# Kernel tuning notes

Measured on AMD Instinct MI355X. Metric: run time of the kernel, lower is better.

The kernel has to match this reference:

```python
import jax, jax.numpy as jnp
import numpy as np
import math

D_MODEL = 256
D_STATE = 16
DT_RANK = math.ceil(D_MODEL / 16)  # 16
WINDOW = 8
B, S = 2, 1024
LN_EPS = 1e-5


def setup_inputs() -> dict:
    key = jax.random.key(0)
    ks = jax.random.split(key, 24)
    d, n, r = D_MODEL, D_STATE, DT_RANK
    sc = lambda fan_in: 1.0 / math.sqrt(fan_in)
    inp = {
        "x": jax.random.normal(ks[0], (B, S, d), jnp.float32),
        # SelectiveSSM params
        "A_log": jnp.log(jnp.abs(jax.random.normal(ks[1], (d, n))) + 1e-4),
        "W_xproj": jax.random.normal(ks[2], (d, r + n)) * sc(d),
        "W_dt": jax.random.normal(ks[3], (r, d)) * sc(r),
        "b_dt": jnp.zeros((d,)),
        "W_C": jax.random.normal(ks[4], (d, n)) * sc(d),
        # LinearAttentionPathway params
        "Wq": jax.random.normal(ks[5], (d, d)) * sc(d),
        "Wk": jax.random.normal(ks[6], (d, d)) * sc(d),
        "Wv": jax.random.normal(ks[7], (d, d)) * sc(d),
        "Wo": jax.random.normal(ks[8], (d, d)) * sc(d),
        "omega": jax.random.normal(ks[9], (d, d)) * 0.5,  # RFF frequencies (buffer)
        # EntropyGate net: Linear(2d+1 -> d), SiLU, Linear(d -> d), Sigmoid
        "Wg1": jax.random.normal(ks[10], (2 * d + 1, d)) * sc(2 * d + 1),
        "bg1": jnp.zeros((d,)),
        "Wg2": jax.random.normal(ks[11], (d, d)) * sc(d),
        "bg2": jnp.zeros((d,)),
        # LayerNorms
        "ln1_g": jnp.ones((d,)), "ln1_b": jnp.zeros((d,)),
        "ln2_g": jnp.ones((d,)), "ln2_b": jnp.zeros((d,)),
        # FFN (dropout is identity in eval)
        "Wf1": jax.random.normal(ks[12], (d, 4 * d)) * sc(d),
        "bf1": jnp.zeros((4 * d,)),
        "Wf2": jax.random.normal(ks[13], (4 * d, d)) * sc(4 * d),
        "bf2": jnp.zeros((d,)),
    }
    return inp


def _layernorm(x, g, b):
    mu = jnp.mean(x, axis=-1, keepdims=True)
    var = jnp.mean((x - mu) ** 2, axis=-1, keepdims=True)
    return (x - mu) / jnp.sqrt(var + LN_EPS) * g + b


def _ssm(x, A_log, W_xproj, W_dt, b_dt, W_C):
    b, s, d = x.shape
    A = -jnp.exp(A_log)                                   # (d, n)
    xp = x @ W_xproj                                      # (b, s, r+n)
    delta = jax.nn.softplus(xp[..., :DT_RANK] @ W_dt + b_dt)  # (b, s, d)
    Bt = xp[..., DT_RANK:]                                # (b, s, n)
    Ct = x @ W_C                                          # (b, s, n)

    def step(h, ins):
        dlt, B_, C_, x_ = ins                             # (b,d),(b,n),(b,n),(b,d)
        A_bar = jnp.exp(dlt[..., None] * A)               # (b, d, n)
        h = A_bar * h + (dlt * x_)[..., None] * B_[:, None, :]
        y = jnp.einsum('bn,bdn->bd', C_, h)
        return h, y

    xs = (delta.transpose(1, 0, 2), Bt.transpose(1, 0, 2),
          Ct.transpose(1, 0, 2), x.transpose(1, 0, 2))
    h0 = jnp.zeros((b, d, D_STATE), x.dtype)
    _, ys = jax.lax.scan(step, h0, xs)                    # (s, b, d)
    return ys.transpose(1, 0, 2)


def _rff(x, omega):
    proj = x @ omega
    scale = math.sqrt(2.0 / D_MODEL)
    return scale * jnp.concatenate([jnp.cos(proj), jnp.sin(proj)], axis=-1)


def _linear_attn(x, Wq, Wk, Wv, Wo, omega):
    b, s, d = x.shape
    Qp = _rff(x @ Wq, omega)                              # (b, s, 2d)
    Kp = _rff(x @ Wk, omega)                              # (b, s, 2d)
    V = x @ Wv                                            # (b, s, d)
    f = 2 * d

    def step(carry, ins):
        Sm, Z = carry                                     # (b,f,d), (b,f)
        q, k, v = ins
        Sm = Sm + k[..., None] * v[:, None, :]
        Z = Z + k
        num = jnp.einsum('bf,bfd->bd', q, Sm)
        den = jnp.sum(q * Z, axis=-1, keepdims=True)
        return (Sm, Z), num / (den + 1e-6)

    xs = (Qp.transpose(1, 0, 2), Kp.transpose(1, 0, 2), V.transpose(1, 0, 2))
    carry0 = (jnp.zeros((b, f, d), x.dtype), jnp.zeros((b, f), x.dtype))
    _, ys = jax.lax.scan(step, carry0, xs)                # (s, b, d)
    return ys.transpose(1, 0, 2) @ Wo


def _entropy(x):
    # H_t over trailing window of token L2-norms; softmax over window.
    m = jnp.linalg.norm(x, axis=-1)                       # (b, s)
    mp = jnp.pad(m, ((0, 0), (WINDOW - 1, 0)), constant_values=-jnp.inf)
    s = m.shape[1]
    # windows[b, t, w]: norms of positions t-W+1..t (padded with -inf)
    windows = jnp.stack([mp[:, i:i + s] for i in range(WINDOW)], axis=-1)
    p = jax.nn.softmax(windows, axis=-1)                  # -inf pads -> p=0
    H = -jnp.sum(p * (jnp.log(p + 1e-9) / jnp.log(2.0)), axis=-1, keepdims=True)
    return H                                              # (b, s, 1)


def reference(x, A_log, W_xproj, W_dt, b_dt, W_C, Wq, Wk, Wv, Wo, omega,
              Wg1, bg1, Wg2, bg2, ln1_g, ln1_b, ln2_g, ln2_b,
              Wf1, bf1, Wf2, bf2):
    residual = x
    y_ssm = _ssm(x, A_log, W_xproj, W_dt, b_dt, W_C)
    y_attn = _linear_attn(x, Wq, Wk, Wv, Wo, omega)
    H = _entropy(x)
    gate_in = jnp.concatenate([y_ssm, y_attn, H], axis=-1)
    g = jax.nn.sigmoid(jax.nn.silu(gate_in @ Wg1 + bg1) @ Wg2 + bg2)
    y_gated = g * y_ssm + (1.0 - g) * y_attn
    h = _layernorm(residual + y_gated, ln1_g, ln1_b)
    ffn = jax.nn.gelu(h @ Wf1 + bf1, approximate=False) @ Wf2 + bf2
    return _layernorm(h + ffn, ln2_g, ln2_b)
```

## Files before the change

### kernel.cpp

```cpp
#include <hip/hip_runtime.h>
#include <math.h>

typedef unsigned short ushort_t;
typedef unsigned int uint_t;
typedef __attribute__((ext_vector_type(8))) short short8;
typedef __attribute__((ext_vector_type(4))) float f32x4;

#define ACT_NONE     0
#define ACT_SOFTPLUS 1
#define ACT_SILU     2
#define ACT_SIGMOID  3
#define ACT_GELU     4
#define ACT_RFF      5
#define ACT_CAUSAL   6

__device__ __forceinline__ ushort_t f2b(float f) {
    union { float f; uint_t u; } v; v.f = f;
    uint_t u = v.u;
    uint_t r = (u + 0x7FFFu + ((u >> 16) & 1u)) >> 16;
    return (ushort_t)r;
}
__device__ __forceinline__ float b2f(ushort_t h) {
    union { uint_t u; float f; } v; v.u = ((uint_t)h) << 16;
    return v.f;
}
__device__ __forceinline__ void split2(float v, ushort_t& h0, ushort_t& h1) {
    h0 = f2b(v); h1 = f2b(v - b2f(h0));
}
__device__ __forceinline__ void split3(float v, ushort_t& h0, ushort_t& h1, ushort_t& h2) {
    h0 = f2b(v); float r1 = v - b2f(h0);
    h1 = f2b(r1); h2 = f2b(r1 - b2f(h1));
}

__device__ __forceinline__ float fast_erf(float x) {
    float ax = fabsf(x);
    float t = 1.f / (1.f + 0.3275911f * ax);
    float poly = t * (0.254829592f + t * (-0.284496736f + t * (1.421413741f
               + t * (-1.453152027f + t * 1.061405429f))));
    float er = 1.f - poly * __expf(-ax * ax);
    return copysignf(er, x);
}

__device__ __forceinline__ float act_apply(float v, int act) {
    switch (act) {
        case ACT_SOFTPLUS: return v > 0.f ? v + __logf(1.f + __expf(-v)) : __logf(1.f + __expf(v));
        case ACT_SILU:     return v / (1.f + __expf(-v));
        case ACT_SIGMOID:  return 1.f / (1.f + __expf(-v));
        case ACT_GELU:     return 0.5f * v * (1.f + fast_erf(v * 0.7071067811865475f));
        default:           return v;
    }
}

#define LDK2 72
#define TSTRIDE 66

struct GJob {
    const ushort_t *A0, *A1, *A2, *B0, *B1, *B2;
    const float* bias;
    float* outF;
    ushort_t *o0, *o1, *o2, *t0, *t1;
    int lda, ldb, ldo, ldob, colOffB, act, ns, K, N;
    int nx, ny, base, zmod;
    int sAb1, sAb2, sBb1, sBb2, sOb, sObB, sTb;
};

struct SJob {
    const float *x, *delta, *BtCt, *A_log, *hstart;
    float *hend, *Pst;
    ushort_t *giH, *giL;
    int base;
};

template<int NSMAX, int AUXPASS>
__global__ __launch_bounds__(256)
void gemm_multi(GJob J0, GJob J1, GJob J2, GJob J3, GJob J4, SJob S)
{
    __shared__ ushort_t ldsbuf[NSMAX * 2 * 64 * LDK2];
    ushort_t (*sA)[64 * LDK2] = (ushort_t(*)[64 * LDK2])ldsbuf;
    ushort_t (*sB)[64 * LDK2] = (ushort_t(*)[64 * LDK2])(ldsbuf + NSMAX * 64 * LDK2);

    int bid = blockIdx.x;

    if constexpr (AUXPASS != 0) {
        if (bid >= S.base) {
            const int bx2 = bid - S.base;
            const int dblk = bx2 & 15, cc = (bx2 >> 4) & 15, bb2 = bx2 >> 8;
            const int tid2 = threadIdx.x;
            const int nn = tid2 & 15, dl = tid2 >> 4;
            const int dd = dblk * 16 + dl;
            float* sd  = (float*)ldsbuf;
            float* sx2 = sd + 1024;
            float* sB2 = sx2 + 1024;
            float* sC2 = sB2 + 1024;
            #pragma unroll
            for (int it = 0; it < 4; ++it) {
                int i2 = it * 256 + tid2;
                int t2 = i2 >> 4, j2 = i2 & 15;
                long row = (long)bb2 * 1024 + cc * 64 + t2;
                sd[t2 * 16 + j2]  = S.delta[row * 256 + dblk * 16 + j2];
                sx2[t2 * 16 + j2] = S.x[row * 256 + dblk * 16 + j2];
                sB2[t2 * 16 + j2] = S.BtCt[row * 32 + j2];
                if (AUXPASS == 3) sC2[t2 * 16 + j2] = S.BtCt[row * 32 + 16 + j2];
            }
            __syncthreads();
            const float acoef = -__expf(S.A_log[dd * 16 + nn]);
            float h = 0.f, P = 1.f;
            if (AUXPASS == 3) h = S.hstart[((long)(bb2 * 16 + cc) << 12) + dd * 16 + nn];
            for (int t2 = 0; t2 < 64; ++t2) {
                float dlt = sd[t2 * 16 + dl];
                float a2 = __expf(dlt * acoef);
                h = a2 * h + (dlt * sx2[t2 * 16 + dl]) * sB2[t2 * 16 + nn];
                if (AUXPASS == 1) P *= a2;
                if (AUXPASS == 3) {
                    float part = sC2[t2 * 16 + nn] * h;
                    #pragma unroll
                    for (int msk = 8; msk; msk >>= 1) part += __shfl_xor(part, msk, 16);
                    if (nn == 0) {
                        long row = (long)bb2 * 1024 + cc * 64 + t2;
                        ushort_t hh = f2b(part);
                        S.giH[row * 576 + dd] = hh;
                        S.giL[row * 576 + dd] = f2b(part - b2f(hh));
                    }
                }
            }
            if (AUXPASS == 1) {
                long idx = ((long)(bb2 * 16 + cc) << 12) + dd * 16 + nn;
                S.hend[idx] = h;
                S.Pst[idx] = P;
            }
            return;
        }
    }

    GJob J = J0;
    if (J4.nx && bid >= J4.base) J = J4;
    else if (J3.nx && bid >= J3.base) J = J3;
    else if (J2.nx && bid >= J2.base) J = J2;
    else if (J1.nx && bid >= J1.base) J = J1;

    int rel = bid - J.base;
    int perz = J.nx * J.ny;
    int bz = rel / perz; rel -= bz * perz;
    int by = rel / J.nx, bx = rel - by * J.nx;
    int zq = bz / J.zmod, zr = bz - zq * J.zmod;

    const ushort_t* As[3] = {J.A0, J.A1, J.A2};
    const ushort_t* Bs[3] = {J.B0, J.B1, J.B2};
    long offA = (long)zq * J.sAb1 + (long)zr * J.sAb2;
    long offB = (long)zq * J.sBb1 + (long)zr * J.sBb2;
    #pragma unroll
    for (int s = 0; s < NSMAX; ++s) { As[s] += offA; Bs[s] += offB; }
    float* outF = J.outF ? J.outF + (long)bz * J.sOb : nullptr;
    ushort_t* o0 = J.o0 ? J.o0 + (long)bz * J.sObB : nullptr;
    ushort_t* o1 = J.o1 ? J.o1 + (long)bz * J.sObB : nullptr;
    ushort_t* o2 = J.o2 ? J.o2 + (long)bz * J.sObB : nullptr;

    const int m0 = by * 64, n0 = bx * 64;
    const int tid = threadIdx.x, lane = tid & 63, wid = tid >> 6;
    const int wr = (wid >> 1) * 32, wc = (wid & 1) * 32;
    const int lr = lane & 15, lk = (lane >> 4) * 8;
    const int rS = tid >> 3, c8 = (tid & 7) * 8;

    uint4 rA[NSMAX][2], rB[NSMAX][2];

    auto LOAD = [&](int k0) {
        #pragma unroll
        for (int s = 0; s < NSMAX; ++s) if (s < J.ns) {
            #pragma unroll
            for (int p = 0; p < 2; ++p) {
                rA[s][p] = *(const uint4*)(As[s] + (long)(m0 + rS + 32 * p) * J.lda + k0 + c8);
                rB[s][p] = *(const uint4*)(Bs[s] + (long)(n0 + rS + 32 * p) * J.ldb + k0 + c8);
            }
        }
    };
    auto STORE = [&]() {
        #pragma unroll
        for (int s = 0; s < NSMAX; ++s) if (s < J.ns) {
            #pragma unroll
            for (int p = 0; p < 2; ++p) {
                *(uint4*)&sA[s][(rS + 32 * p) * LDK2 + c8] = rA[s][p];
                *(uint4*)&sB[s][(rS + 32 * p) * LDK2 + c8] = rB[s][p];
            }
        }
    };

    f32x4 acc[2][2];
    #pragma unroll
    for (int i = 0; i < 2; ++i)
        #pragma unroll
        for (int j = 0; j < 2; ++j)
            acc[i][j] = (f32x4){0.f, 0.f, 0.f, 0.f};

    const int niter = J.K >> 6;
    LOAD(0);
    for (int it = 0; it < niter; ++it) {
        if (it) __syncthreads();
        STORE();
        __syncthreads();
        if (it + 1 < niter) LOAD((it + 1) << 6);
        #pragma unroll
        for (int ks = 0; ks < 2; ++ks) {
            short8 af[NSMAX][2], bg[NSMAX][2];
            #pragma unroll
            for (int s = 0; s < NSMAX; ++s) if (s < J.ns) {
                af[s][0] = *(const short8*)&sA[s][(wr + lr) * LDK2 + ks * 32 + lk];
                af[s][1] = *(const short8*)&sA[s][(wr + 16 + lr) * LDK2 + ks * 32 + lk];
                bg[s][0] = *(const short8*)&sB[s][(wc + lr) * LDK2 + ks * 32 + lk];
                bg[s][1] = *(const short8*)&sB[s][(wc + 16 + lr) * LDK2 + ks * 32 + lk];
            }
            #pragma unroll
            for (int i = 0; i < 2; ++i) {
                #pragma unroll
                for (int j = 0; j < 2; ++j) {
                    acc[i][j] = __builtin_amdgcn_mfma_f32_16x16x32_bf16(af[0][i], bg[0][j], acc[i][j], 0, 0, 0);
                    if constexpr (NSMAX >= 2) if (J.ns >= 2) {
                        acc[i][j] = __builtin_amdgcn_mfma_f32_16x16x32_bf16(af[0][i], bg[1][j], acc[i][j], 0, 0, 0);
                        acc[i][j] = __builtin_amdgcn_mfma_f32_16x16x32_bf16(af[1][i], bg[0][j], acc[i][j], 0, 0, 0);
                    }
                    if constexpr (NSMAX >= 3) if (J.ns >= 3) {
                        acc[i][j] = __builtin_amdgcn_mfma_f32_16x16x32_bf16(af[0][i], bg[2][j], acc[i][j], 0, 0, 0);
                        acc[i][j] = __builtin_amdgcn_mfma_f32_16x16x32_bf16(af[1][i], bg[1][j], acc[i][j], 0, 0, 0);
                        acc[i][j] = __builtin_amdgcn_mfma_f32_16x16x32_bf16(af[2][i], bg[0][j], acc[i][j], 0, 0, 0);
                    }
                }
            }
        }
    }

    ushort_t* sAf = &sA[0][0];
    ushort_t* sBf = &sB[0][0];
    const bool hasT = (J.t0 != nullptr);
    if (hasT) __syncthreads();

    #pragma unroll
    for (int i = 0; i < 2; ++i) {
        #pragma unroll
        for (int j = 0; j < 2; ++j) {
            #pragma unroll
            for (int rr = 0; rr < 4; ++rr) {
                int rl2 = wr + i * 16 + (lane >> 4) * 4 + rr;
                int cl2 = wc + j * 16 + lr;
                int row = m0 + rl2;
                int col = n0 + cl2;
                if (col >= J.N) continue;
                float v = acc[i][j][rr];
                if (J.bias) v += J.bias[col];
                if (J.act == ACT_RFF) {
                    const float sc = 0.08838834764831845f;
                    float sv_, cv_;
                    __sincosf(v, &sv_, &cv_);
                    float cv = sc * cv_, sv = sc * sv_;
                    ushort_t ch = f2b(cv), sh = f2b(sv);
                    ushort_t cL = f2b(cv - b2f(ch)), sL = f2b(sv - b2f(sh));
                    long oc = (long)row * J.ldob + col, os = oc + J.N;
                    o0[oc] = ch; o0[os] = sh;
                    o1[oc] = cL; o1[os] = sL;
                    if (hasT) {
                        sAf[cl2 * TSTRIDE + rl2] = ch;
                        sAf[4224 + cl2 * TSTRIDE + rl2] = cL;
                        sBf[cl2 * TSTRIDE + rl2] = sh;
                        sBf[4224 + cl2 * TSTRIDE + rl2] = sL;
                    }
                    continue;
                }
                if (J.act == ACT_CAUSAL) { if (col > row) v = 0.f; }
                else v = act_apply(v, J.act);
                if (outF) outF[(long)row * J.ldo + col] = v;
                if (o0) {
                    long o = (long)row * J.ldob + J.colOffB + col;
                    ushort_t h0 = f2b(v); o0[o] = h0;
                    if (o1) {
                        float r1 = v - b2f(h0);
                        ushort_t h1 = f2b(r1); o1[o] = h1;
                        if (o2) o2[o] = f2b(r1 - b2f(h1));
                    }
                }
                if (hasT) {
                    ushort_t h0 = f2b(v);
                    sAf[cl2 * TSTRIDE + rl2] = h0;
                    sAf[4224 + cl2 * TSTRIDE + rl2] = f2b(v - b2f(h0));
                }
            }
        }
    }

    if (hasT) {
        __syncthreads();
        int bb = m0 >> 10, tl0 = m0 & 1023;
        int cl = tid >> 2, seg = tid & 3;
        int ngroups = (J.act == ACT_RFF) ? 2 : 1;
        for (int g = 0; g < ngroups; ++g) {
            const ushort_t* th = (g ? sBf : sAf) + cl * TSTRIDE + seg * 16;
            const ushort_t* tl = th + 4224;
            long gcol = (long)(n0 + cl) + (long)g * J.N;
            long addr = (long)bb * J.sTb + gcol * 1024 + tl0 + seg * 16;
            uint_t wh[8], wl[8];
            #pragma unroll
            for (int k2 = 0; k2 < 8; ++k2) {
                wh[k2] = (uint_t)th[2 * k2] | ((uint_t)th[2 * k2 + 1] << 16);
                wl[k2] = (uint_t)tl[2 * k2] | ((uint_t)tl[2 * k2 + 1] << 16);
            }
            *(uint4*)(J.t0 + addr)     = *(uint4*)&wh[0];
            *(uint4*)(J.t0 + addr + 8) = *(uint4*)&wh[4];
            *(uint4*)(J.t1 + addr)     = *(uint4*)&wl[0];
            *(uint4*)(J.t1 + addr + 8) = *(uint4*)&wl[4];
        }
    }
}

#define CONV_BLKS 6400
__global__ __launch_bounds__(256)
void convert_kernel(const float* __restrict__ x, const float* __restrict__ Wxp,
                    const float* __restrict__ Wdt, const float* __restrict__ Wc,
                    const float* __restrict__ Wq, const float* __restrict__ Wk,
                    const float* __restrict__ Wv, const float* __restrict__ Wo,
                    const float* __restrict__ omega, const float* __restrict__ Wg1,
                    const float* __restrict__ Wg2, const float* __restrict__ Wf1,
                    const float* __restrict__ Wf2,
                    ushort_t* x0, ushort_t* x1, ushort_t* x2,
                    ushort_t* omT0, ushort_t* omT1, ushort_t* omT2,
                    ushort_t* Wq0, ushort_t* Wq1, ushort_t* Wq2,
                    ushort_t* Wk0, ushort_t* Wk1, ushort_t* Wk2,
                    ushort_t* WvT0, ushort_t* WvT1, ushort_t* WoT0, ushort_t* WoT1,
                    ushort_t* Wg1T0, ushort_t* Wg1T1, ushort_t* Wg2T0, ushort_t* Wg2T1,
                    ushort_t* Wf1T, ushort_t* Wf2T,
                    ushort_t* WdtT0, ushort_t* WdtT1, ushort_t* WxpP0, ushort_t* WxpP1,
                    ushort_t* WbcT0, ushort_t* WbcT1, float* mbuf)
{
    if (blockIdx.x >= CONV_BLKS) {
        int w = threadIdx.x >> 6, lane = threadIdx.x & 63;
        int token = (blockIdx.x - CONV_BLKS) * 4 + w;
        const float4 v = ((const float4*)(x + (long)token * 256))[lane];
        float s = v.x * v.x + v.y * v.y + v.z * v.z + v.w * v.w;
        #pragma unroll
        for (int msk = 32; msk; msk >>= 1) s += __shfl_xor(s, msk, 64);
        if (lane == 0) mbuf[token] = sqrtf(s);
        return;
    }
    int i = blockIdx.x * 256 + threadIdx.x;
    if (i < 524288) { split3(x[i], x0[i], x1[i], x2[i]); return; }
    i -= 524288;
    if (i < 65536) { int r = i >> 8, c = i & 255; split3(omega[c * 256 + r], omT0[i], omT1[i], omT2[i]); return; }
    i -= 65536;
    if (i < 65536) { split3(Wq[i], Wq0[i], Wq1[i], Wq2[i]); return; }
    i -= 65536;
    if (i < 65536) { split3(Wk[i], Wk0[i], Wk1[i], Wk2[i]); return; }
    i -= 65536;
    if (i < 65536) { int r = i >> 8, c = i & 255; split2(Wv[c * 256 + r], WvT0[i], WvT1[i]); return; }
    i -= 65536;
    if (i < 65536) { int r = i >> 8, c = i & 255; split2(Wo[c * 256 + r], WoT0[i], WoT1[i]); return; }
    i -= 65536;
    if (i < 147456) { int r = i / 576, c = i - r * 576;
                      float v = (c < 513) ? Wg1[c * 256 + r] : 0.f;
                      split2(v, Wg1T0[i], Wg1T1[i]); return; }
    i -= 147456;
    if (i < 65536) { int r = i >> 8, c = i & 255; split2(Wg2[c * 256 + r], Wg2T0[i], Wg2T1[i]); return; }
    i -= 65536;
    if (i < 262144) { int r = i >> 8, c = i & 255; Wf1T[i] = f2b(Wf1[c * 1024 + r]); return; }
    i -= 262144;
    if (i < 262144) { int r = i >> 10, c = i & 1023; Wf2T[i] = f2b(Wf2[c * 256 + r]); return; }
    i -= 262144;
    if (i < 16384) { int m = i >> 6, k = i & 63;
                     float v = (k < 16) ? Wdt[k * 256 + m] : 0.f;
                     split2(v, WdtT0[i], WdtT1[i]); return; }
    i -= 16384;
    if (i < 16384) { int n = i >> 6, k = i & 63;
                     float v = (k < 16) ? Wxp[n * 32 + k] : 0.f;
                     split2(v, WxpP0[i], WxpP1[i]); return; }
    i -= 16384;
    if (i < 16384) { int r = i >> 8, c = i & 255;
                     float v = (r < 16) ? Wxp[c * 32 + 16 + r] : ((r < 32) ? Wc[c * 16 + (r - 16)] : 0.f);
                     split2(v, WbcT0[i], WbcT1[i]); return; }
}

__global__ void scan_mix(const float* __restrict__ hend, const float* __restrict__ Pst,
                         float* __restrict__ hstart,
                         const ushort_t* __restrict__ Kh, const ushort_t* __restrict__ Kl,
                         float* __restrict__ dzc,
                         const float* __restrict__ dST,
                         ushort_t* __restrict__ STh, ushort_t* __restrict__ STl)
{
    int gb = blockIdx.x;
    if (gb < 32) {
        int tid = gb * 256 + threadIdx.x;
        int b = tid >> 12;
        int dn = tid & 4095;
        float hs = 0.f;
        for (int c = 0; c < 16; ++c) {
            long idx = ((long)(b * 16 + c) << 12) + dn;
            hstart[idx] = hs;
            hs = Pst[idx] * hs + hend[idx];
        }
    } else if (gb < 64) {
        int idx = (gb - 32) * 256 + threadIdx.x;
        int bc = idx >> 9, f = idx & 511;
        float s = 0.f;
        for (int t = 0; t < 128; ++t) {
            long i = ((long)bc * 128 + t) * 512 + f;
            s += b2f(Kh[i]) + b2f(Kl[i]);
        }
        dzc[(long)bc * 512 + f] = s;
    } else {
        int t = (gb - 64) * 256 + threadIdx.x;
        int b = t >> 17;
        int df = t & 131071;
        float acc = 0.f;
        for (int c = 0; c < 8; ++c) {
            long idx = (long)(b * 8 + c) * 131072 + df;
            float v = dST[idx];
            ushort_t h = f2b(acc);
            STh[idx] = h;
            STl[idx] = f2b(acc - b2f(h));
            acc += v;
        }
    }
}

__global__ void attn_finish(const float* __restrict__ scores,
                            const ushort_t* __restrict__ Qh, const ushort_t* __restrict__ Ql,
                            const float* __restrict__ dzc,
                            const float* __restrict__ numA, const float* __restrict__ numB,
                            const float* __restrict__ mbuf,
                            ushort_t* __restrict__ yh, ushort_t* __restrict__ yl,
                            ushort_t* __restrict__ giH, ushort_t* __restrict__ giL)
{
    int token = blockIdx.x;
    int b = token >> 10, tloc = token & 1023;
    int c = tloc >> 7, tin = tloc & 127;
    int bc = b * 8 + c;
    int lane = threadIdx.x;
    const float* srow = scores + ((long)bc * 128 + tin) * 128;
    float s = srow[lane] + srow[lane + 64];
    const ushort_t* qh = Qh + (long)token * 512;
    const ushort_t* ql = Ql + (long)token * 512;
    float q[8];
    #pragma unroll
    for (int j = 0; j < 8; ++j) {
        int f = lane + 64 * j;
        q[j] = b2f(qh[f]) + b2f(ql[f]);
    }
    for (int c2 = 0; c2 < c; ++c2) {
        const float* z = dzc + (long)(b * 8 + c2) * 512;
        #pragma unroll
        for (int j = 0; j < 8; ++j) s += q[j] * z[lane + 64 * j];
    }
    #pragma unroll
    for (int m = 32; m; m >>= 1) s += __shfl_xor(s, m, 64);
    float inv = 1.f / (s + 1e-6f);
    const float* na = numA + (long)token * 256;
    const float* nb = numB + (long)token * 256;
    #pragma unroll
    for (int j = 0; j < 4; ++j) {
        int idx = lane + 64 * j;
        float v = (na[idx] + nb[idx]) * inv;
        ushort_t h = f2b(v);
        yh[(long)token * 256 + idx] = h;
        yl[(long)token * 256 + idx] = f2b(v - b2f(h));
    }
    if (lane == 0) {
        float w[8];
        #pragma unroll
        for (int i = 0; i < 8; ++i) {
            int idx = tloc - 7 + i;
            w[i] = (idx >= 0) ? mbuf[b * 1024 + idx] : -1e30f;
        }
        float mx = w[0];
        #pragma unroll
        for (int i = 1; i < 8; ++i) mx = fmaxf(mx, w[i]);
        float e[8], sum = 0.f;
        #pragma unroll
        for (int i = 0; i < 8; ++i) { e[i] = __expf(w[i] - mx); sum += e[i]; }
        float invs = 1.f / sum, Hv = 0.f;
        #pragma unroll
        for (int i = 0; i < 8; ++i) {
            float p = e[i] * invs;
            Hv -= p * __logf(p + 1e-9f);
        }
        float H = Hv * 1.4426950408889634f;
        ushort_t hh = f2b(H);
        giH[(long)token * 576 + 512] = hh;
        giL[(long)token * 576 + 512] = f2b(H - b2f(hh));
    }
    if (lane < 63) {
        giH[(long)token * 576 + 513 + lane] = 0;
        giL[(long)token * 576 + 513 + lane] = 0;
    }
}

__global__ __launch_bounds__(256)
void ln1_kernel(const float* __restrict__ x, const float* __restrict__ g,
                const ushort_t* __restrict__ giH, const ushort_t* __restrict__ giL,
                const float* __restrict__ gamma, const float* __restrict__ beta,
                float* __restrict__ outF, ushort_t* __restrict__ outB)
{
    __shared__ float red[8];
    long t = blockIdx.x;
    int i = threadIdx.x;
    long idx = t * 256 + i;
    float yssm  = b2f(giH[t * 576 + i])       + b2f(giL[t * 576 + i]);
    float yattn = b2f(giH[t * 576 + 256 + i]) + b2f(giL[t * 576 + 256 + i]);
    float gv = g[idx];
    float v = x[idx] + gv * yssm + (1.f - gv) * yattn;
    float s = v;
    #pragma unroll
    for (int m = 32; m; m >>= 1) s += __shfl_xor(s, m, 64);
    if ((i & 63) == 0) red[i >> 6] = s;
    __syncthreads();
    float mu = (red[0] + red[1] + red[2] + red[3]) * (1.f / 256.f);
    float dv = v - mu;
    float s2 = dv * dv;
    #pragma unroll
    for (int m = 32; m; m >>= 1) s2 += __shfl_xor(s2, m, 64);
    if ((i & 63) == 0) red[4 + (i >> 6)] = s2;
    __syncthreads();
    float var = (red[4] + red[5] + red[6] + red[7]) * (1.f / 256.f);
    float o = dv * rsqrtf(var + 1e-5f) * gamma[i] + beta[i];
    outF[idx] = o;
    outB[idx] = f2b(o);
}

__global__ __launch_bounds__(256)
void ln2_kernel(const float* __restrict__ h, const float* __restrict__ f2,
                const float* __restrict__ gamma, const float* __restrict__ beta,
                float* __restrict__ out)
{
    __shared__ float red[8];
    long t = blockIdx.x;
    int i = threadIdx.x;
    long idx = t * 256 + i;
    float v = h[idx] + f2[idx];
    float s = v;
    #pragma unroll
    for (int m = 32; m; m >>= 1) s += __shfl_xor(s, m, 64);
    if ((i & 63) == 0) red[i >> 6] = s;
    __syncthreads();
    float mu = (red[0] + red[1] + red[2] + red[3]) * (1.f / 256.f);
    float dv = v - mu;
    float s2 = dv * dv;
    #pragma unroll
    for (int m = 32; m; m >>= 1) s2 += __shfl_xor(s2, m, 64);
    if ((i & 63) == 0) red[4 + (i >> 6)] = s2;
    __syncthreads();
    float var = (red[4] + red[5] + red[6] + red[7]) * (1.f / 256.f);
    out[idx] = dv * rsqrtf(var + 1e-5f) * gamma[i] + beta[i];
}


extern "C" void kernel_launch(void* const* d_in, const int* in_sizes, int n_in,
                              void* d_out, int out_size, void* d_ws, size_t ws_size,
                              hipStream_t stream)
{
    const float* x       = (const float*)d_in[0];
    const float* A_log   = (const float*)d_in[1];
    const float* W_xproj = (const float*)d_in[2];
    const float* W_dt    = (const float*)d_in[3];
    const float* b_dt    = (const float*)d_in[4];
    const float* W_C     = (const float*)d_in[5];
    const float* Wq      = (const float*)d_in[6];
    const float* Wk      = (const float*)d_in[7];
    const float* Wv      = (const float*)d_in[8];
    const float* Wo      = (const float*)d_in[9];
    const float* omega   = (const float*)d_in[10];
    const float* Wg1     = (const float*)d_in[11];
    const float* bg1     = (const float*)d_in[12];
    const float* Wg2     = (const float*)d_in[13];
    const float* bg2     = (const float*)d_in[14];
    const float* ln1_g   = (const float*)d_in[15];
    const float* ln1_b   = (const float*)d_in[16];
    const float* ln2_g   = (const float*)d_in[17];
    const float* ln2_b   = (const float*)d_in[18];
    const float* Wf1     = (const float*)d_in[19];
    const float* bf1     = (const float*)d_in[20];
    const float* Wf2     = (const float*)d_in[21];
    const float* bf2     = (const float*)d_in[22];

    char* B = (char*)d_ws;
    float* out = (float*)d_out;
    if (ws_size < (size_t)42778624) return;

    ushort_t* x0      = (ushort_t*)(B + 0);
    ushort_t* x1      = (ushort_t*)(B + 1048576);
    ushort_t* x2      = (ushort_t*)(B + 2097152);
    ushort_t* Qp_hi   = (ushort_t*)(B + 3145728);
    ushort_t* Qp_lo   = (ushort_t*)(B + 5242880);
    ushort_t* Kp_hi   = (ushort_t*)(B + 7340032);
    ushort_t* Kp_lo   = (ushort_t*)(B + 9437184);
    ushort_t* KpT_hi  = (ushort_t*)(B + 11534336);
    ushort_t* KpT_lo  = (ushort_t*)(B + 13631488);
    ushort_t* VT_hi   = (ushort_t*)(B + 15728640);
    ushort_t* VT_lo   = (ushort_t*)(B + 16777216);
    float*    dST_f   = (float*)(B + 17825792);
    float*    delta_f = (float*)(B + 26214400);
    float*    BtCt_f  = (float*)(B + 28311552);
    ushort_t* Wg1T0   = (ushort_t*)(B + 28573696);
    ushort_t* Wg1T1   = (ushort_t*)(B + 28868608);
    ushort_t* Wf1T    = (ushort_t*)(B + 29163520);
    ushort_t* Wf2T    = (ushort_t*)(B + 29687808);
    ushort_t* WxdT0   = (ushort_t*)(B + 30212096);
    ushort_t* WxdT1   = (ushort_t*)(B + 30343168);
    ushort_t* WvT0    = (ushort_t*)(B + 30474240);
    ushort_t* WvT1    = (ushort_t*)(B + 30605312);
    ushort_t* WoT0    = (ushort_t*)(B + 30736384);
    ushort_t* WoT1    = (ushort_t*)(B + 30867456);
    ushort_t* Wg2T0   = (ushort_t*)(B + 30998528);
    ushort_t* Wg2T1   = (ushort_t*)(B + 31129600);
    ushort_t* WdtT0   = (ushort_t*)(B + 31260672);
    ushort_t* WdtT1   = (ushort_t*)(B + 31293440);
    ushort_t* WxpP0   = (ushort_t*)(B + 31326208);
    ushort_t* WxpP1   = (ushort_t*)(B + 31358976);
    ushort_t* WbcT0   = (ushort_t*)(B + 31391744);
    ushort_t* WbcT1   = (ushort_t*)(B + 31424512);
    float*    mbuf    = (float*)(B + 31457280);
    float*    dzc     = (float*)(B + 31465472);
    ushort_t* gatein_hi = (ushort_t*)(B + 31498240);
    ushort_t* gatein_lo = (ushort_t*)(B + 33857536);
    ushort_t* ST_lo   = (ushort_t*)(B + 36216832);
    float*    scores_f  = (float*)(B + 40411136);
    ushort_t* scores_hi = (ushort_t*)(B + 41459712);
    ushort_t* scores_lo = (ushort_t*)(B + 41984000);
    ushort_t* omT0  = (ushort_t*)(B + 17825792);
    ushort_t* omT1  = (ushort_t*)(B + 17956864);
    ushort_t* omT2  = (ushort_t*)(B + 18087936);
    ushort_t* Wq0   = (ushort_t*)(B + 18219008);
    ushort_t* Wq1   = (ushort_t*)(B + 18350080);
    ushort_t* Wq2   = (ushort_t*)(B + 18481152);
    ushort_t* Wk0   = (ushort_t*)(B + 18612224);
    ushort_t* Wk1   = (ushort_t*)(B + 18743296);
    ushort_t* Wk2   = (ushort_t*)(B + 18874368);
    ushort_t* WqoT0 = (ushort_t*)(B + 19005440);
    ushort_t* WqoT1 = (ushort_t*)(B + 19136512);
    ushort_t* WqoT2 = (ushort_t*)(B + 19267584);
    ushort_t* WkoT0 = (ushort_t*)(B + 19398656);
    ushort_t* WkoT1 = (ushort_t*)(B + 19529728);
    ushort_t* WkoT2 = (ushort_t*)(B + 19660800);
    ushort_t* ST_hi = (ushort_t*)(B + 11534336);
    float*    hend   = (float*)(B + 0);
    float*    Pst    = (float*)(B + 524288);
    float*    hstart = (float*)(B + 1048576);
    float*    numA_f = (float*)(B + 17825792);
    float*    numB_f = (float*)(B + 19922944);
    ushort_t* g1_hi  = (ushort_t*)(B + 22020096);
    ushort_t* g1_lo  = (ushort_t*)(B + 23068672);
    float*    gbuf_f = (float*)(B + 24117248);
    ushort_t* ypre_hi = (ushort_t*)(B + 7340032);
    ushort_t* ypre_lo = (ushort_t*)(B + 8388608);
    float*    hbuf_f  = (float*)(B + 11534336);
    ushort_t* hbuf_b  = (ushort_t*)(B + 13631488);
    ushort_t* ffn1_b  = (ushort_t*)(B + 3145728);
    float*    ffn2_f  = (float*)(B + 15728640);

    dim3 T256(256);
    GJob jz{};
    SJob sz{};

    convert_kernel<<<dim3(CONV_BLKS + 512), T256, 0, stream>>>(x, W_xproj, W_dt, W_C,
        Wq, Wk, Wv, Wo, omega, Wg1, Wg2, Wf1, Wf2,
        x0, x1, x2, omT0, omT1, omT2, Wq0, Wq1, Wq2, Wk0, Wk1, Wk2,
        WvT0, WvT1, WoT0, WoT1, Wg1T0, Wg1T1, Wg2T0, Wg2T1, Wf1T, Wf2T,
        WdtT0, WdtT1, WxpP0, WxpP1, WbcT0, WbcT1, mbuf);

    {
        GJob a{}; a.A0=omT0; a.A1=omT1; a.A2=omT2; a.B0=Wq0; a.B1=Wq1; a.B2=Wq2;
        a.o0=WqoT0; a.o1=WqoT1; a.o2=WqoT2; a.lda=256; a.ldb=256; a.ldob=256;
        a.act=ACT_NONE; a.ns=3; a.K=256; a.N=256; a.nx=4; a.ny=4; a.base=0; a.zmod=1;
        GJob b = a; b.B0=Wk0; b.B1=Wk1; b.B2=Wk2; b.o0=WkoT0; b.o1=WkoT1; b.o2=WkoT2; b.base=16;
        GJob c{}; c.A0=WdtT0; c.A1=WdtT1; c.B0=WxpP0; c.B1=WxpP1;
        c.o0=WxdT0; c.o1=WxdT1; c.lda=64; c.ldb=64; c.ldob=256;
        c.act=ACT_NONE; c.ns=2; c.K=64; c.N=256; c.nx=4; c.ny=4; c.base=32; c.zmod=1;
        gemm_multi<3,0><<<dim3(48), T256, 0, stream>>>(a, b, c, jz, jz, sz);
    }
    {
        GJob v{}; v.A0=x0; v.A1=x1; v.B0=WvT0; v.B1=WvT1;
        v.t0=VT_hi; v.t1=VT_lo; v.sTb=262144;
        v.lda=256; v.ldb=256; v.act=ACT_NONE; v.ns=2; v.K=256; v.N=256;
        v.nx=4; v.ny=32; v.base=0; v.zmod=1;
        GJob q{}; q.A0=x0; q.A1=x1; q.A2=x2; q.B0=WqoT0; q.B1=WqoT1; q.B2=WqoT2;
        q.o0=Qp_hi; q.o1=Qp_lo; q.lda=256; q.ldb=256; q.ldob=512;
        q.act=ACT_RFF; q.ns=3; q.K=256; q.N=256; q.nx=4; q.ny=32; q.base=128; q.zmod=1;
        GJob k = q; k.B0=WkoT0; k.B1=WkoT1; k.B2=WkoT2; k.o0=Kp_hi; k.o1=Kp_lo;
        k.t0=KpT_hi; k.t1=KpT_lo; k.sTb=524288; k.base=256;
        GJob bc{}; bc.A0=x0; bc.A1=x1; bc.B0=WbcT0; bc.B1=WbcT1;
        bc.outF=BtCt_f; bc.lda=256; bc.ldb=256; bc.ldo=32;
        bc.act=ACT_NONE; bc.ns=2; bc.K=256; bc.N=32; bc.nx=1; bc.ny=32; bc.base=384; bc.zmod=1;
        GJob dl{}; dl.A0=x0; dl.A1=x1; dl.B0=WxdT0; dl.B1=WxdT1; dl.bias=b_dt;
        dl.outF=delta_f; dl.lda=256; dl.ldb=256; dl.ldo=256;
        dl.act=ACT_SOFTPLUS; dl.ns=2; dl.K=256; dl.N=256; dl.nx=4; dl.ny=32; dl.base=416; dl.zmod=1;
        gemm_multi<3,0><<<dim3(544), T256, 0, stream>>>(v, q, k, bc, dl, sz);
    }
    {
        GJob d{}; d.A0=VT_hi; d.A1=VT_lo; d.B0=KpT_hi; d.B1=KpT_lo;
        d.outF=dST_f; d.lda=1024; d.ldb=1024; d.ldo=512;
        d.act=ACT_NONE; d.ns=2; d.K=128; d.N=512; d.nx=8; d.ny=4; d.base=0; d.zmod=8;
        d.sAb1=262144; d.sAb2=128; d.sBb1=524288; d.sBb2=128; d.sOb=131072;
        GJob s{}; s.A0=Qp_hi; s.A1=Qp_lo; s.B0=Kp_hi; s.B1=Kp_lo;
        s.outF=scores_f; s.o0=scores_hi; s.o1=scores_lo;
        s.lda=512; s.ldb=512; s.ldo=128; s.ldob=128;
        s.act=ACT_CAUSAL; s.ns=2; s.K=512; s.N=128; s.nx=2; s.ny=2; s.base=512; s.zmod=1;
        s.sAb1=65536; s.sBb1=65536; s.sOb=16384; s.sObB=16384;
        SJob s1{}; s1.x=x; s1.delta=delta_f; s1.BtCt=BtCt_f; s1.A_log=A_log;
        s1.hend=hend; s1.Pst=Pst; s1.base=576;
        gemm_multi<2,1><<<dim3(1088), T256, 0, stream>>>(d, s, jz, jz, jz, s1);
    }
    scan_mix<<<dim3(1088), T256, 0, stream>>>(hend, Pst, hstart, Kp_hi, Kp_lo, dzc,
                                              dST_f, ST_hi, ST_lo);
    {
        GJob a{}; a.A0=scores_hi; a.A1=scores_lo; a.B0=VT_hi; a.B1=VT_lo;
        a.outF=numA_f; a.lda=128; a.ldb=1024; a.ldo=256;
        a.act=ACT_NONE; a.ns=2; a.K=128; a.N=256; a.nx=4; a.ny=2; a.base=0; a.zmod=8;
        a.sAb1=131072; a.sAb2=16384; a.sBb1=262144; a.sBb2=128; a.sOb=32768;
        GJob b{}; b.A0=Qp_hi; b.A1=Qp_lo; b.B0=ST_hi; b.B1=ST_lo;
        b.outF=numB_f; b.lda=512; b.ldb=512; b.ldo=256;
        b.act=ACT_NONE; b.ns=2; b.K=512; b.N=256; b.nx=4; b.ny=2; b.base=128; b.zmod=1;
        b.sAb1=65536; b.sBb1=131072; b.sOb=32768;
        SJob s3{}; s3.x=x; s3.delta=delta_f; s3.BtCt=BtCt_f; s3.A_log=A_log;
        s3.hstart=hstart; s3.giH=gatein_hi; s3.giL=gatein_lo; s3.base=256;
        gemm_multi<2,3><<<dim3(768), T256, 0, stream>>>(a, b, jz, jz, jz, s3);
    }
    attn_finish<<<dim3(2048), dim3(64), 0, stream>>>(scores_f, Qp_hi, Qp_lo, dzc,
        numA_f, numB_f, mbuf, ypre_hi, ypre_lo, gatein_hi, gatein_lo);
    {
        GJob w{}; w.A0=ypre_hi; w.A1=ypre_lo; w.B0=WoT0; w.B1=WoT1;
        w.o0=gatein_hi; w.o1=gatein_lo; w.colOffB=256;
        w.lda=256; w.ldb=256; w.ldob=576;
        w.act=ACT_NONE; w.ns=2; w.K=256; w.N=256; w.nx=4; w.ny=32; w.base=0; w.zmod=1;
        gemm_multi<2,0><<<dim3(128), T256, 0, stream>>>(w, jz, jz, jz, jz, sz);
    }
    {
        GJob g{}; g.A0=gatein_hi; g.A1=gatein_lo; g.B0=Wg1T0; g.B1=Wg1T1; g.bias=bg1;
        g.o0=g1_hi; g.o1=g1_lo; g.lda=576; g.ldb=576; g.ldob=256;
        g.act=ACT_SILU; g.ns=2; g.K=576; g.N=256; g.nx=4; g.ny=32; g.base=0; g.zmod=1;
        gemm_multi<2,0><<<dim3(128), T256, 0, stream>>>(g, jz, jz, jz, jz, sz);
    }
    {
        GJob g{}; g.A0=g1_hi; g.A1=g1_lo; g.B0=Wg2T0; g.B1=Wg2T1; g.bias=bg2;
        g.outF=gbuf_f; g.lda=256; g.ldb=256; g.ldo=256;
        g.act=ACT_SIGMOID; g.ns=2; g.K=256; g.N=256; g.nx=4; g.ny=32; g.base=0; g.zmod=1;
        gemm_multi<2,0><<<dim3(128), T256, 0, stream>>>(g, jz, jz, jz, jz, sz);
    }
    ln1_kernel<<<dim3(2048), T256, 0, stream>>>(x, gbuf_f, gatein_hi, gatein_lo, ln1_g, ln1_b, hbuf_f, hbuf_b);
    {
        GJob f{}; f.A0=hbuf_b; f.B0=Wf1T; f.bias=bf1;
        f.o0=ffn1_b; f.lda=256; f.ldb=256; f.ldob=1024;
        f.act=ACT_GELU; f.ns=1; f.K=256; f.N=1024; f.nx=16; f.ny=32; f.base=0; f.zmod=1;
        gemm_multi<1,0><<<dim3(512), T256, 0, stream>>>(f, jz, jz, jz, jz, sz);
    }
    {
        GJob f{}; f.A0=ffn1_b; f.B0=Wf2T; f.bias=bf2;
        f.outF=ffn2_f; f.lda=1024; f.ldb=1024; f.ldo=256;
        f.act=ACT_NONE; f.ns=1; f.K=1024; f.N=256; f.nx=4; f.ny=32; f.base=0; f.zmod=1;
        gemm_multi<1,0><<<dim3(128), T256, 0, stream>>>(f, jz, jz, jz, jz, sz);
    }
    ln2_kernel<<<dim3(2048), T256, 0, stream>>>(hbuf_f, ffn2_f, ln2_g, ln2_b, out);
}
```

Before: 311.8 us.

## Fuse all stages into one cooperative persistent kernel with grid syncs

Replaces the chain of separate kernel launches (convert, multi-GEMMs, scans, attention finish, gate GEMMs, layernorms, FFN) with a single cooperative persistent kernel. Blocks loop over virtual block IDs in each stage, and stages are separated by grid.sync(). This targets launch overhead and inter-kernel gaps across roughly a dozen dependent launches. In exchange it limits the grid to 256 or 512 resident blocks, which may reduce parallelism for stages that had many more blocks. Each grid-wide barrier also has its own cost.

```diff
diff --git a/kernel.cpp b/kernel.cpp
--- a/kernel.cpp
+++ b/kernel.cpp
@@ -1,5 +1,8 @@
 #include <hip/hip_runtime.h>
+#include <hip/hip_cooperative_groups.h>
 #include <math.h>
+
+namespace cg = cooperative_groups;
 
 typedef unsigned short ushort_t;
 typedef unsigned int uint_t;
@@ -64,79 +67,14 @@
     int sAb1, sAb2, sBb1, sBb2, sOb, sObB, sTb;
 };
 
-struct SJob {
-    const float *x, *delta, *BtCt, *A_log, *hstart;
-    float *hend, *Pst;
-    ushort_t *giH, *giL;
-    int base;
-};
-
-template<int NSMAX, int AUXPASS>
-__global__ __launch_bounds__(256)
-void gemm_multi(GJob J0, GJob J1, GJob J2, GJob J3, GJob J4, SJob S)
+template<int NSMAX>
+__device__ __noinline__ void gemm_body(int bid, const GJob* js, int nj, ushort_t* ldsbuf)
 {
-    __shared__ ushort_t ldsbuf[NSMAX * 2 * 64 * LDK2];
     ushort_t (*sA)[64 * LDK2] = (ushort_t(*)[64 * LDK2])ldsbuf;
     ushort_t (*sB)[64 * LDK2] = (ushort_t(*)[64 * LDK2])(ldsbuf + NSMAX * 64 * LDK2);
 
-    int bid = blockIdx.x;
-
-    if constexpr (AUXPASS != 0) {
-        if (bid >= S.base) {
-            const int bx2 = bid - S.base;
-            const int dblk = bx2 & 15, cc = (bx2 >> 4) & 15, bb2 = bx2 >> 8;
-            const int tid2 = threadIdx.x;
-            const int nn = tid2 & 15, dl = tid2 >> 4;
-            const int dd = dblk * 16 + dl;
-            float* sd  = (float*)ldsbuf;
-            float* sx2 = sd + 1024;
-            float* sB2 = sx2 + 1024;
-            float* sC2 = sB2 + 1024;
-            #pragma unroll
-            for (int it = 0; it < 4; ++it) {
-                int i2 = it * 256 + tid2;
-                int t2 = i2 >> 4, j2 = i2 & 15;
-                long row = (long)bb2 * 1024 + cc * 64 + t2;
-                sd[t2 * 16 + j2]  = S.delta[row * 256 + dblk * 16 + j2];
-                sx2[t2 * 16 + j2] = S.x[row * 256 + dblk * 16 + j2];
-                sB2[t2 * 16 + j2] = S.BtCt[row * 32 + j2];
-                if (AUXPASS == 3) sC2[t2 * 16 + j2] = S.BtCt[row * 32 + 16 + j2];
-            }
-            __syncthreads();
-            const float acoef = -__expf(S.A_log[dd * 16 + nn]);
-            float h = 0.f, P = 1.f;
-            if (AUXPASS == 3) h = S.hstart[((long)(bb2 * 16 + cc) << 12) + dd * 16 + nn];
-            for (int t2 = 0; t2 < 64; ++t2) {
-                float dlt = sd[t2 * 16 + dl];
-                float a2 = __expf(dlt * acoef);
-                h = a2 * h + (dlt * sx2[t2 * 16 + dl]) * sB2[t2 * 16 + nn];
-                if (AUXPASS == 1) P *= a2;
-                if (AUXPASS == 3) {
-                    float part = sC2[t2 * 16 + nn] * h;
-                    #pragma unroll
-                    for (int msk = 8; msk; msk >>= 1) part += __shfl_xor(part, msk, 16);
-                    if (nn == 0) {
-                        long row = (long)bb2 * 1024 + cc * 64 + t2;
-                        ushort_t hh = f2b(part);
-                        S.giH[row * 576 + dd] = hh;
-                        S.giL[row * 576 + dd] = f2b(part - b2f(hh));
-                    }
-                }
-            }
-            if (AUXPASS == 1) {
-                long idx = ((long)(bb2 * 16 + cc) << 12) + dd * 16 + nn;
-                S.hend[idx] = h;
-                S.Pst[idx] = P;
-            }
-            return;
-        }
-    }
-
-    GJob J = J0;
-    if (J4.nx && bid >= J4.base) J = J4;
-    else if (J3.nx && bid >= J3.base) J = J3;
-    else if (J2.nx && bid >= J2.base) J = J2;
-    else if (J1.nx && bid >= J1.base) J = J1;
+    GJob J = js[0];
+    for (int j = nj - 1; j > 0; --j) if (bid >= js[j].base) { J = js[j]; break; }
 
     int rel = bid - J.base;
     int perz = J.nx * J.ny;
@@ -306,358 +244,165 @@
             *(uint4*)(J.t1 + addr + 8) = *(uint4*)&wl[4];
         }
     }
-}
-
-#define CONV_BLKS 6400
-__global__ __launch_bounds__(256)
-void convert_kernel(const float* __restrict__ x, const float* __restrict__ Wxp,
-                    const float* __restrict__ Wdt, const float* __restrict__ Wc,
-                    const float* __restrict__ Wq, const float* __restrict__ Wk,
-                    const float* __restrict__ Wv, const float* __restrict__ Wo,
-                    const float* __restrict__ omega, const float* __restrict__ Wg1,
-                    const float* __restrict__ Wg2, const float* __restrict__ Wf1,
-                    const float* __restrict__ Wf2,
-                    ushort_t* x0, ushort_t* x1, ushort_t* x2,
-                    ushort_t* omT0, ushort_t* omT1, ushort_t* omT2,
-                    ushort_t* Wq0, ushort_t* Wq1, ushort_t* Wq2,
-                    ushort_t* Wk0, ushort_t* Wk1, ushort_t* Wk2,
-                    ushort_t* WvT0, ushort_t* WvT1, ushort_t* WoT0, ushort_t* WoT1,
-                    ushort_t* Wg1T0, ushort_t* Wg1T1, ushort_t* Wg2T0, ushort_t* Wg2T1,
-                    ushort_t* Wf1T, ushort_t* Wf2T,
-                    ushort_t* WdtT0, ushort_t* WdtT1, ushort_t* WxpP0, ushort_t* WxpP1,
-                    ushort_t* WbcT0, ushort_t* WbcT1, float* mbuf)
+    __syncthreads();
+}
+
+template<int PASS>
+__device__ __noinline__ void ssm_body(int bx2, const float* x, const float* delta,
+                                      const float* BtCt, const float* A_log,
+                                      float* hend, float* Pst, const float* hstart,
+                                      ushort_t* giH, ushort_t* giL, ushort_t* ldsbuf)
 {
-    if (blockIdx.x >= CONV_BLKS) {
-        int w = threadIdx.x >> 6, lane = threadIdx.x & 63;
-        int token = (blockIdx.x - CONV_BLKS) * 4 + w;
-        const float4 v = ((const float4*)(x + (long)token * 256))[lane];
-        float s = v.x * v.x + v.y * v.y + v.z * v.z + v.w * v.w;
-        #pragma unroll
-        for (int msk = 32; msk; msk >>= 1) s += __shfl_xor(s, msk, 64);
-        if (lane == 0) mbuf[token] = sqrtf(s);
-        return;
-    }
-    int i = blockIdx.x * 256 + threadIdx.x;
-    if (i < 524288) { split3(x[i], x0[i], x1[i], x2[i]); return; }
-    i -= 524288;
-    if (i < 65536) { int r = i >> 8, c = i & 255; split3(omega[c * 256 + r], omT0[i], omT1[i], omT2[i]); return; }
-    i -= 65536;
-    if (i < 65536) { split3(Wq[i], Wq0[i], Wq1[i], Wq2[i]); return; }
-    i -= 65536;
-    if (i < 65536) { split3(Wk[i], Wk0[i], Wk1[i], Wk2[i]); return; }
-    i -= 65536;
-    if (i < 65536) { int r = i >> 8, c = i & 255; split2(Wv[c * 256 + r], WvT0[i], WvT1[i]); return; }
-    i -= 65536;
-    if (i < 65536) { int r = i >> 8, c = i & 255; split2(Wo[c * 256 + r], WoT0[i], WoT1[i]); return; }
-    i -= 65536;
-    if (i < 147456) { int r = i / 576, c = i - r * 576;
-                      float v = (c < 513) ? Wg1[c * 256 + r] : 0.f;
-                      split2(v, Wg1T0[i], Wg1T1[i]); return; }
-    i -= 147456;
-    if (i < 65536) { int r = i >> 8, c = i & 255; split2(Wg2[c * 256 + r], Wg2T0[i], Wg2T1[i]); return; }
-    i -= 65536;
-    if (i < 262144) { int r = i >> 8, c = i & 255; Wf1T[i] = f2b(Wf1[c * 1024 + r]); return; }
-    i -= 262144;
-    if (i < 262144) { int r = i >> 10, c = i & 1023; Wf2T[i] = f2b(Wf2[c * 256 + r]); return; }
-    i -= 262144;
-    if (i < 16384) { int m = i >> 6, k = i & 63;
-                     float v = (k < 16) ? Wdt[k * 256 + m] : 0.f;
-                     split2(v, WdtT0[i], WdtT1[i]); return; }
-    i -= 16384;
-    if (i < 16384) { int n = i >> 6, k = i & 63;
-                     float v = (k < 16) ? Wxp[n * 32 + k] : 0.f;
-                     split2(v, WxpP0[i], WxpP1[i]); return; }
-    i -= 16384;
-    if (i < 16384) { int r = i >> 8, c = i & 255;
-                     float v = (r < 16) ? Wxp[c * 32 + 16 + r] : ((r < 32) ? Wc[c * 16 + (r - 16)] : 0.f);
-                     split2(v, WbcT0[i], WbcT1[i]); return; }
-}
-
-__global__ void scan_mix(const float* __restrict__ hend, const float* __restrict__ Pst,
-                         float* __restrict__ hstart,
-                         const ushort_t* __restrict__ Kh, const ushort_t* __restrict__ Kl,
-                         float* __restrict__ dzc,
-                         const float* __restrict__ dST,
-                         ushort_t* __restrict__ STh, ushort_t* __restrict__ STl)
+    const int dblk = bx2 & 15, cc = (bx2 >> 4) & 15, bb2 = bx2 >> 8;
+    const int tid2 = threadIdx.x;
+    const int nn = tid2 & 15, dl = tid2 >> 4;
+    const int dd = dblk * 16 + dl;
+    float* sd  = (float*)ldsbuf;
+    float* sx2 = sd + 1024;
+    float* sB2 = sx2 + 1024;
+    float* sC2 = sB2 + 1024;
+    #pragma unroll
+    for (int it = 0; it < 4; ++it) {
+        int i2 = it * 256 + tid2;
+        int t2 = i2 >> 4, j2 = i2 & 15;
+        long row = (long)bb2 * 1024 + cc * 64 + t2;
+        sd[t2 * 16 + j2]  = delta[row * 256 + dblk * 16 + j2];
+        sx2[t2 * 16 + j2] = x[row * 256 + dblk * 16 + j2];
+        sB2[t2 * 16 + j2] = BtCt[row * 32 + j2];
+        if (PASS == 3) sC2[t2 * 16 + j2] = BtCt[row * 32 + 16 + j2];
+    }
+    __syncthreads();
+    const float acoef = -__expf(A_log[dd * 16 + nn]);
+    float h = 0.f, P = 1.f;
+    if (PASS == 3) h = hstart[((long)(bb2 * 16 + cc) << 12) + dd * 16 + nn];
+    for (int t2 = 0; t2 < 64; ++t2) {
+        float dlt = sd[t2 * 16 + dl];
+        float a2 = __expf(dlt * acoef);
+        h = a2 * h + (dlt * sx2[t2 * 16 + dl]) * sB2[t2 * 16 + nn];
+        if (PASS == 1) P *= a2;
+        if (PASS == 3) {
+            float part = sC2[t2 * 16 + nn] * h;
+            #pragma unroll
+            for (int msk = 8; msk; msk >>= 1) part += __shfl_xor(part, msk, 16);
+            if (nn == 0) {
+                long row = (long)bb2 * 1024 + cc * 64 + t2;
+                ushort_t hh = f2b(part);
+                giH[row * 576 + dd] = hh;
+                giL[row * 576 + dd] = f2b(part - b2f(hh));
+            }
+        }
+    }
+    if (PASS == 1) {
+        long idx = ((long)(bb2 * 16 + cc) << 12) + dd * 16 + nn;
+        hend[idx] = h;
+        Pst[idx] = P;
+    }
+    __syncthreads();
+}
+
+struct MegaArgs {
+    const float *x, *A_log, *Wxp, *Wdt, *b_dt, *Wc, *Wq, *Wk, *Wv, *Wo, *omega,
+                *Wg1, *bg1, *Wg2, *bg2, *ln1g, *ln1b, *ln2g, *ln2b,
+                *Wf1, *bf1, *Wf2, *bf2;
+    char* B;
+    float* out;
+};
+
+#define PUS(off) ((ushort_t*)(A.B + (off)))
+#define PF(off)  ((float*)(A.B + (off)))
+
+__global__ void __launch_bounds__(256)
+mega(MegaArgs A)
 {
-    int gb = blockIdx.x;
-    if (gb < 32) {
-        int tid = gb * 256 + threadIdx.x;
-        int b = tid >> 12;
-        int dn = tid & 4095;
-        float hs = 0.f;
-        for (int c = 0; c < 16; ++c) {
-            long idx = ((long)(b * 16 + c) << 12) + dn;
-            hstart[idx] = hs;
-            hs = Pst[idx] * hs + hend[idx];
-        }
-    } else if (gb < 64) {
-        int idx = (gb - 32) * 256 + threadIdx.x;
-        int bc = idx >> 9, f = idx & 511;
-        float s = 0.f;
-        for (int t = 0; t < 128; ++t) {
-            long i = ((long)bc * 128 + t) * 512 + f;
-            s += b2f(Kh[i]) + b2f(Kl[i]);
-        }
-        dzc[(long)bc * 512 + f] = s;
-    } else {
-        int t = (gb - 64) * 256 + threadIdx.x;
-        int b = t >> 17;
-        int df = t & 131071;
-        float acc = 0.f;
-        for (int c = 0; c < 8; ++c) {
-            long idx = (long)(b * 8 + c) * 131072 + df;
-            float v = dST[idx];
-            ushort_t h = f2b(acc);
-            STh[idx] = h;
-            STl[idx] = f2b(acc - b2f(h));
-            acc += v;
-        }
-    }
-}
-
-__global__ void attn_finish(const float* __restrict__ scores,
-                            const ushort_t* __restrict__ Qh, const ushort_t* __restrict__ Ql,
-                            const float* __restrict__ dzc,
-                            const float* __restrict__ numA, const float* __restrict__ numB,
-                            const float* __restrict__ mbuf,
-                            ushort_t* __restrict__ yh, ushort_t* __restrict__ yl,
-                            ushort_t* __restrict__ giH, ushort_t* __restrict__ giL)
-{
-    int token = blockIdx.x;
-    int b = token >> 10, tloc = token & 1023;
-    int c = tloc >> 7, tin = tloc & 127;
-    int bc = b * 8 + c;
-    int lane = threadIdx.x;
-    const float* srow = scores + ((long)bc * 128 + tin) * 128;
-    float s = srow[lane] + srow[lane + 64];
-    const ushort_t* qh = Qh + (long)token * 512;
-    const ushort_t* ql = Ql + (long)token * 512;
-    float q[8];
-    #pragma unroll
-    for (int j = 0; j < 8; ++j) {
-        int f = lane + 64 * j;
-        q[j] = b2f(qh[f]) + b2f(ql[f]);
-    }
-    for (int c2 = 0; c2 < c; ++c2) {
-        const float* z = dzc + (long)(b * 8 + c2) * 512;
-        #pragma unroll
-        for (int j = 0; j < 8; ++j) s += q[j] * z[lane + 64 * j];
-    }
-    #pragma unroll
-    for (int m = 32; m; m >>= 1) s += __shfl_xor(s, m, 64);
-    float inv = 1.f / (s + 1e-6f);
-    const float* na = numA + (long)token * 256;
-    const float* nb = numB + (long)token * 256;
-    #pragma unroll
-    for (int j = 0; j < 4; ++j) {
-        int idx = lane + 64 * j;
-        float v = (na[idx] + nb[idx]) * inv;
-        ushort_t h = f2b(v);
-        yh[(long)token * 256 + idx] = h;
-        yl[(long)token * 256 + idx] = f2b(v - b2f(h));
-    }
-    if (lane == 0) {
-        float w[8];
-        #pragma unroll
-        for (int i = 0; i < 8; ++i) {
-            int idx = tloc - 7 + i;
-            w[i] = (idx >= 0) ? mbuf[b * 1024 + idx] : -1e30f;
-        }
-        float mx = w[0];
-        #pragma unroll
-        for (int i = 1; i < 8; ++i) mx = fmaxf(mx, w[i]);
-        float e[8], sum = 0.f;
-        #pragma unroll
-        for (int i = 0; i < 8; ++i) { e[i] = __expf(w[i] - mx); sum += e[i]; }
-        float invs = 1.f / sum, Hv = 0.f;
-        #pragma unroll
-        for (int i = 0; i < 8; ++i) {
-            float p = e[i] * invs;
-            Hv -= p * __logf(p + 1e-9f);
-        }
-        float H = Hv * 1.4426950408889634f;
-        ushort_t hh = f2b(H);
-        giH[(long)token * 576 + 512] = hh;
-        giL[(long)token * 576 + 512] = f2b(H - b2f(hh));
-    }
-    if (lane < 63) {
-        giH[(long)token * 576 + 513 + lane] = 0;
-        giL[(long)token * 576 + 513 + lane] = 0;
-    }
-}
-
-__global__ __launch_bounds__(256)
-void ln1_kernel(const float* __restrict__ x, const float* __restrict__ g,
-                const ushort_t* __restrict__ giH, const ushort_t* __restrict__ giL,
-                const float* __restrict__ gamma, const float* __restrict__ beta,
-                float* __restrict__ outF, ushort_t* __restrict__ outB)
-{
-    __shared__ float red[8];
-    long t = blockIdx.x;
-    int i = threadIdx.x;
-    long idx = t * 256 + i;
-    float yssm  = b2f(giH[t * 576 + i])       + b2f(giL[t * 576 + i]);
-    float yattn = b2f(giH[t * 576 + 256 + i]) + b2f(giL[t * 576 + 256 + i]);
-    float gv = g[idx];
-    float v = x[idx] + gv * yssm + (1.f - gv) * yattn;
-    float s = v;
-    #pragma unroll
-    for (int m = 32; m; m >>= 1) s += __shfl_xor(s, m, 64);
-    if ((i & 63) == 0) red[i >> 6] = s;
-    __syncthreads();
-    float mu = (red[0] + red[1] + red[2] + red[3]) * (1.f / 256.f);
-    float dv = v - mu;
-    float s2 = dv * dv;
-    #pragma unroll
-    for (int m = 32; m; m >>= 1) s2 += __shfl_xor(s2, m, 64);
-    if ((i & 63) == 0) red[4 + (i >> 6)] = s2;
-    __syncthreads();
-    float var = (red[4] + red[5] + red[6] + red[7]) * (1.f / 256.f);
-    float o = dv * rsqrtf(var + 1e-5f) * gamma[i] + beta[i];
-    outF[idx] = o;
-    outB[idx] = f2b(o);
-}
-
-__global__ __launch_bounds__(256)
-void ln2_kernel(const float* __restrict__ h, const float* __restrict__ f2,
-                const float* __restrict__ gamma, const float* __restrict__ beta,
-                float* __restrict__ out)
-{
-    __shared__ float red[8];
-    long t = blockIdx.x;
-    int i = threadIdx.x;
-    long idx = t * 256 + i;
-    float v = h[idx] + f2[idx];
-    float s = v;
-    #pragma unroll
-    for (int m = 32; m; m >>= 1) s += __shfl_xor(s, m, 64);
-    if ((i & 63) == 0) red[i >> 6] = s;
-    __syncthreads();
-    float mu = (red[0] + red[1] + red[2] + red[3]) * (1.f / 256.f);
-    float dv = v - mu;
-    float s2 = dv * dv;
-    #pragma unroll
-    for (int m = 32; m; m >>= 1) s2 += __shfl_xor(s2, m, 64);
-    if ((i & 63) == 0) red[4 + (i >> 6)] = s2;
-    __syncthreads();
-    float var = (red[4] + red[5] + red[6] + red[7]) * (1.f / 256.f);
-    out[idx] = dv * rsqrtf(var + 1e-5f) * gamma[i] + beta[i];
-}
-
-
-extern "C" void kernel_launch(void* const* d_in, const int* in_sizes, int n_in,
-                              void* d_out, int out_size, void* d_ws, size_t ws_size,
-                              hipStream_t stream)
-{
-    const float* x       = (const float*)d_in[0];
-    const float* A_log   = (const float*)d_in[1];
-    const float* W_xproj = (const float*)d_in[2];
-    const float* W_dt    = (const float*)d_in[3];
-    const float* b_dt    = (const float*)d_in[4];
-    const float* W_C     = (const float*)d_in[5];
-    const float* Wq      = (const float*)d_in[6];
-    const float* Wk      = (const float*)d_in[7];
-    const float* Wv      = (const float*)d_in[8];
-    const float* Wo      = (const float*)d_in[9];
-    const float* omega   = (const float*)d_in[10];
-    const float* Wg1     = (const float*)d_in[11];
-    const float* bg1     = (const float*)d_in[12];
-    const float* Wg2     = (const float*)d_in[13];
-    const float* bg2     = (const float*)d_in[14];
-    const float* ln1_g   = (const float*)d_in[15];
-    const float* ln1_b   = (const float*)d_in[16];
-    const float* ln2_g   = (const float*)d_in[17];
-    const float* ln2_b   = (const float*)d_in[18];
-    const float* Wf1     = (const float*)d_in[19];
-    const float* bf1     = (const float*)d_in[20];
-    const float* Wf2     = (const float*)d_in[21];
-    const float* bf2     = (const float*)d_in[22];
-
-    char* B = (char*)d_ws;
-    float* out = (float*)d_out;
-    if (ws_size < (size_t)42778624) return;
-
-    ushort_t* x0      = (ushort_t*)(B + 0);
-    ushort_t* x1      = (ushort_t*)(B + 1048576);
-    ushort_t* x2      = (ushort_t*)(B + 2097152);
-    ushort_t* Qp_hi   = (ushort_t*)(B + 3145728);
-    ushort_t* Qp_lo   = (ushort_t*)(B + 5242880);
-    ushort_t* Kp_hi   = (ushort_t*)(B + 7340032);
-    ushort_t* Kp_lo   = (ushort_t*)(B + 9437184);
-    ushort_t* KpT_hi  = (ushort_t*)(B + 11534336);
-    ushort_t* KpT_lo  = (ushort_t*)(B + 13631488);
-    ushort_t* VT_hi   = (ushort_t*)(B + 15728640);
-    ushort_t* VT_lo   = (ushort_t*)(B + 16777216);
-    float*    dST_f   = (float*)(B + 17825792);
-    float*    delta_f = (float*)(B + 26214400);
-    float*    BtCt_f  = (float*)(B + 28311552);
-    ushort_t* Wg1T0   = (ushort_t*)(B + 28573696);
-    ushort_t* Wg1T1   = (ushort_t*)(B + 28868608);
-    ushort_t* Wf1T    = (ushort_t*)(B + 29163520);
-    ushort_t* Wf2T    = (ushort_t*)(B + 29687808);
-    ushort_t* WxdT0   = (ushort_t*)(B + 30212096);
-    ushort_t* WxdT1   = (ushort_t*)(B + 30343168);
-    ushort_t* WvT0    = (ushort_t*)(B + 30474240);
-    ushort_t* WvT1    = (ushort_t*)(B + 30605312);
-    ushort_t* WoT0    = (ushort_t*)(B + 30736384);
-    ushort_t* WoT1    = (ushort_t*)(B + 30867456);
-    ushort_t* Wg2T0   = (ushort_t*)(B + 30998528);
-    ushort_t* Wg2T1   = (ushort_t*)(B + 31129600);
-    ushort_t* WdtT0   = (ushort_t*)(B + 31260672);
-    ushort_t* WdtT1   = (ushort_t*)(B + 31293440);
-    ushort_t* WxpP0   = (ushort_t*)(B + 31326208);
-    ushort_t* WxpP1   = (ushort_t*)(B + 31358976);
-    ushort_t* WbcT0   = (ushort_t*)(B + 31391744);
-    ushort_t* WbcT1   = (ushort_t*)(B + 31424512);
-    float*    mbuf    = (float*)(B + 31457280);
-    float*    dzc     = (float*)(B + 31465472);
-    ushort_t* gatein_hi = (ushort_t*)(B + 31498240);
-    ushort_t* gatein_lo = (ushort_t*)(B + 33857536);
-    ushort_t* ST_lo   = (ushort_t*)(B + 36216832);
-    float*    scores_f  = (float*)(B + 40411136);
-    ushort_t* scores_hi = (ushort_t*)(B + 41459712);
-    ushort_t* scores_lo = (ushort_t*)(B + 41984000);
-    ushort_t* omT0  = (ushort_t*)(B + 17825792);
-    ushort_t* omT1  = (ushort_t*)(B + 17956864);
-    ushort_t* omT2  = (ushort_t*)(B + 18087936);
-    ushort_t* Wq0   = (ushort_t*)(B + 18219008);
-    ushort_t* Wq1   = (ushort_t*)(B + 18350080);
-    ushort_t* Wq2   = (ushort_t*)(B + 18481152);
-    ushort_t* Wk0   = (ushort_t*)(B + 18612224);
-    ushort_t* Wk1   = (ushort_t*)(B + 18743296);
-    ushort_t* Wk2   = (ushort_t*)(B + 18874368);
-    ushort_t* WqoT0 = (ushort_t*)(B + 19005440);
-    ushort_t* WqoT1 = (ushort_t*)(B + 19136512);
-    ushort_t* WqoT2 = (ushort_t*)(B + 19267584);
-    ushort_t* WkoT0 = (ushort_t*)(B + 19398656);
-    ushort_t* WkoT1 = (ushort_t*)(B + 19529728);
-    ushort_t* WkoT2 = (ushort_t*)(B + 19660800);
-    ushort_t* ST_hi = (ushort_t*)(B + 11534336);
-    float*    hend   = (float*)(B + 0);
-    float*    Pst    = (float*)(B + 524288);
-    float*    hstart = (float*)(B + 1048576);
-    float*    numA_f = (float*)(B + 17825792);
-    float*    numB_f = (float*)(B + 19922944);
-    ushort_t* g1_hi  = (ushort_t*)(B + 22020096);
-    ushort_t* g1_lo  = (ushort_t*)(B + 23068672);
-    float*    gbuf_f = (float*)(B + 24117248);
-    ushort_t* ypre_hi = (ushort_t*)(B + 7340032);
-    ushort_t* ypre_lo = (ushort_t*)(B + 8388608);
-    float*    hbuf_f  = (float*)(B + 11534336);
-    ushort_t* hbuf_b  = (ushort_t*)(B + 13631488);
-    ushort_t* ffn1_b  = (ushort_t*)(B + 3145728);
-    float*    ffn2_f  = (float*)(B + 15728640);
-
-    dim3 T256(256);
-    GJob jz{};
-    SJob sz{};
-
-    convert_kernel<<<dim3(CONV_BLKS + 512), T256, 0, stream>>>(x, W_xproj, W_dt, W_C,
-        Wq, Wk, Wv, Wo, omega, Wg1, Wg2, Wf1, Wf2,
-        x0, x1, x2, omT0, omT1, omT2, Wq0, Wq1, Wq2, Wk0, Wk1, Wk2,
-        WvT0, WvT1, WoT0, WoT1, Wg1T0, Wg1T1, Wg2T0, Wg2T1, Wf1T, Wf2T,
-        WdtT0, WdtT1, WxpP0, WxpP1, WbcT0, WbcT1, mbuf);
+    cg::grid_group grid = cg::this_grid();
+    __shared__ ushort_t ldsbuf[3 * 2 * 64 * LDK2];
+    const int NB = gridDim.x;
+    const int bid = blockIdx.x;
+    const int tid = threadIdx.x;
+
+    ushort_t *x0 = PUS(0), *x1 = PUS(1048576), *x2 = PUS(2097152);
+    ushort_t *Qp_hi = PUS(3145728), *Qp_lo = PUS(5242880);
+    ushort_t *Kp_hi = PUS(7340032), *Kp_lo = PUS(9437184);
+    ushort_t *KpT_hi = PUS(11534336), *KpT_lo = PUS(13631488);
+    ushort_t *VT_hi = PUS(15728640), *VT_lo = PUS(16777216);
+    float *dST_f = PF(17825792), *delta_f = PF(26214400), *BtCt_f = PF(28311552);
+    ushort_t *Wg1T0 = PUS(28573696), *Wg1T1 = PUS(28868608);
+    ushort_t *Wf1T = PUS(29163520), *Wf2T = PUS(29687808);
+    ushort_t *WxdT0 = PUS(30212096), *WxdT1 = PUS(30343168);
+    ushort_t *WvT0 = PUS(30474240), *WvT1 = PUS(30605312);
+    ushort_t *WoT0 = PUS(30736384), *WoT1 = PUS(30867456);
+    ushort_t *Wg2T0 = PUS(30998528), *Wg2T1 = PUS(31129600);
+    ushort_t *WdtT0 = PUS(31260672), *WdtT1 = PUS(31293440);
+    ushort_t *WxpP0 = PUS(31326208), *WxpP1 = PUS(31358976);
+    ushort_t *WbcT0 = PUS(31391744), *WbcT1 = PUS(31424512);
+    float *mbuf = PF(31457280), *dzc = PF(31465472);
+    ushort_t *gatein_hi = PUS(31498240), *gatein_lo = PUS(33857536);
+    ushort_t *ST_lo = PUS(36216832);
+    float *scores_f = PF(40411136);
+    ushort_t *scores_hi = PUS(41459712), *scores_lo = PUS(41984000);
+    ushort_t *omT0 = PUS(17825792), *omT1 = PUS(17956864), *omT2 = PUS(18087936);
+    ushort_t *Wq0 = PUS(18219008), *Wq1 = PUS(18350080), *Wq2 = PUS(18481152);
+    ushort_t *Wk0 = PUS(18612224), *Wk1 = PUS(18743296), *Wk2 = PUS(18874368);
+    ushort_t *WqoT0 = PUS(19005440), *WqoT1 = PUS(19136512), *WqoT2 = PUS(19267584);
+    ushort_t *WkoT0 = PUS(19398656), *WkoT1 = PUS(19529728), *WkoT2 = PUS(19660800);
+    ushort_t *ST_hi = PUS(11534336);
+    float *hend = PF(0), *Pst = PF(524288), *hstart = PF(1048576);
+    float *numA_f = PF(17825792), *numB_f = PF(19922944);
+    ushort_t *g1_hi = PUS(22020096), *g1_lo = PUS(23068672);
+    float *gbuf_f = PF(24117248);
+    ushort_t *ypre_hi = PUS(7340032), *ypre_lo = PUS(8388608);
+    float *hbuf_f = PF(11534336);
+    ushort_t *hbuf_b = PUS(13631488);
+    ushort_t *ffn1_b = PUS(3145728);
+    float *ffn2_f = PF(15728640);
+
+    for (int v = bid; v < 6912; v += NB) {
+        if (v >= 6400) {
+            int w = tid >> 6, lane = tid & 63;
+            int token = (v - 6400) * 4 + w;
+            const float4 vv = ((const float4*)(A.x + (long)token * 256))[lane];
+            float s = vv.x * vv.x + vv.y * vv.y + vv.z * vv.z + vv.w * vv.w;
+            #pragma unroll
+            for (int msk = 32; msk; msk >>= 1) s += __shfl_xor(s, msk, 64);
+            if (lane == 0) mbuf[token] = sqrtf(s);
+            continue;
+        }
+        int i = v * 256 + tid;
+        if (i < 524288) { split3(A.x[i], x0[i], x1[i], x2[i]); continue; }
+        i -= 524288;
+        if (i < 65536) { int r = i >> 8, c = i & 255; split3(A.omega[c * 256 + r], omT0[i], omT1[i], omT2[i]); continue; }
+        i -= 65536;
+        if (i < 65536) { split3(A.Wq[i], Wq0[i], Wq1[i], Wq2[i]); continue; }
+        i -= 65536;
+        if (i < 65536) { split3(A.Wk[i], Wk0[i], Wk1[i], Wk2[i]); continue; }
+        i -= 65536;
+        if (i < 65536) { int r = i >> 8, c = i & 255; split2(A.Wv[c * 256 + r], WvT0[i], WvT1[i]); continue; }
+        i -= 65536;
+        if (i < 65536) { int r = i >> 8, c = i & 255; split2(A.Wo[c * 256 + r], WoT0[i], WoT1[i]); continue; }
+        i -= 65536;
+        if (i < 147456) { int r = i / 576, c = i - r * 576;
+                          float vv = (c < 513) ? A.Wg1[c * 256 + r] : 0.f;
+                          split2(vv, Wg1T0[i], Wg1T1[i]); continue; }
+        i -= 147456;
+        if (i < 65536) { int r = i >> 8, c = i & 255; split2(A.Wg2[c * 256 + r], Wg2T0[i], Wg2T1[i]); continue; }
+        i -= 65536;
+        if (i < 262144) { int r = i >> 8, c = i & 255; Wf1T[i] = f2b(A.Wf1[c * 1024 + r]); continue; }
+        i -= 262144;
+        if (i < 262144) { int r = i >> 10, c = i & 1023; Wf2T[i] = f2b(A.Wf2[c * 256 + r]); continue; }
+        i -= 262144;
+        if (i < 16384) { int m = i >> 6, k = i & 63;
+                         float vv = (k < 16) ? A.Wdt[k * 256 + m] : 0.f;
+                         split2(vv, WdtT0[i], WdtT1[i]); continue; }
+        i -= 16384;
+        if (i < 16384) { int n = i >> 6, k = i & 63;
+                         float vv = (k < 16) ? A.Wxp[n * 32 + k] : 0.f;
+                         split2(vv, WxpP0[i], WxpP1[i]); continue; }
+        i -= 16384;
+        if (i < 16384) { int r = i >> 8, c = i & 255;
+                         float vv = (r < 16) ? A.Wxp[c * 32 + 16 + r] : ((r < 32) ? A.Wc[c * 16 + (r - 16)] : 0.f);
+                         split2(vv, WbcT0[i], WbcT1[i]); continue; }
+    }
+    grid.sync();
 
     {
         GJob a{}; a.A0=omT0; a.A1=omT1; a.A2=omT2; a.B0=Wq0; a.B1=Wq1; a.B2=Wq2;
@@ -667,8 +412,11 @@
         GJob c{}; c.A0=WdtT0; c.A1=WdtT1; c.B0=WxpP0; c.B1=WxpP1;
         c.o0=WxdT0; c.o1=WxdT1; c.lda=64; c.ldb=64; c.ldob=256;
         c.act=ACT_NONE; c.ns=2; c.K=64; c.N=256; c.nx=4; c.ny=4; c.base=32; c.zmod=1;
-        gemm_multi<3,0><<<dim3(48), T256, 0, stream>>>(a, b, c, jz, jz, sz);
-    }
+        GJob js[3] = {a, b, c};
+        for (int v = bid; v < 48; v += NB) gemm_body<3>(v, js, 3, ldsbuf);
+    }
+    grid.sync();
+
     {
         GJob v{}; v.A0=x0; v.A1=x1; v.B0=WvT0; v.B1=WvT1;
         v.t0=VT_hi; v.t1=VT_lo; v.sTb=262144;
@@ -682,11 +430,14 @@
         GJob bc{}; bc.A0=x0; bc.A1=x1; bc.B0=WbcT0; bc.B1=WbcT1;
         bc.outF=BtCt_f; bc.lda=256; bc.ldb=256; bc.ldo=32;
         bc.act=ACT_NONE; bc.ns=2; bc.K=256; bc.N=32; bc.nx=1; bc.ny=32; bc.base=384; bc.zmod=1;
-        GJob dl{}; dl.A0=x0; dl.A1=x1; dl.B0=WxdT0; dl.B1=WxdT1; dl.bias=b_dt;
+        GJob dl{}; dl.A0=x0; dl.A1=x1; dl.B0=WxdT0; dl.B1=WxdT1; dl.bias=A.b_dt;
         dl.outF=delta_f; dl.lda=256; dl.ldb=256; dl.ldo=256;
         dl.act=ACT_SOFTPLUS; dl.ns=2; dl.K=256; dl.N=256; dl.nx=4; dl.ny=32; dl.base=416; dl.zmod=1;
-        gemm_multi<3,0><<<dim3(544), T256, 0, stream>>>(v, q, k, bc, dl, sz);
-    }
+        GJob js[5] = {v, q, k, bc, dl};
+        for (int vb = bid; vb < 544; vb += NB) gemm_body<3>(vb, js, 5, ldsbuf);
+    }
+    grid.sync();
+
     {
         GJob d{}; d.A0=VT_hi; d.A1=VT_lo; d.B0=KpT_hi; d.B1=KpT_lo;
         d.outF=dST_f; d.lda=1024; d.ldb=1024; d.ldo=512;
@@ -697,12 +448,54 @@
         s.lda=512; s.ldb=512; s.ldo=128; s.ldob=128;
         s.act=ACT_CAUSAL; s.ns=2; s.K=512; s.N=128; s.nx=2; s.ny=2; s.base=512; s.zmod=1;
         s.sAb1=65536; s.sBb1=65536; s.sOb=16384; s.sObB=16384;
-        SJob s1{}; s1.x=x; s1.delta=delta_f; s1.BtCt=BtCt_f; s1.A_log=A_log;
-        s1.hend=hend; s1.Pst=Pst; s1.base=576;
-        gemm_multi<2,1><<<dim3(1088), T256, 0, stream>>>(d, s, jz, jz, jz, s1);
-    }
-    scan_mix<<<dim3(1088), T256, 0, stream>>>(hend, Pst, hstart, Kp_hi, Kp_lo, dzc,
-                                              dST_f, ST_hi, ST_lo);
+        GJob js[2] = {d, s};
+        for (int vb = bid; vb < 1088; vb += NB) {
+            if (vb >= 576)
+                ssm_body<1>(vb - 576, A.x, delta_f, BtCt_f, A.A_log, hend, Pst,
+                            nullptr, nullptr, nullptr, ldsbuf);
+            else
+                gemm_body<2>(vb, js, 2, ldsbuf);
+        }
+    }
+    grid.sync();
+
+    for (int gb = bid; gb < 1088; gb += NB) {
+        if (gb < 32) {
+            int t = gb * 256 + tid;
+            int b = t >> 12;
+            int dn = t & 4095;
+            float hs = 0.f;
+            for (int c = 0; c < 16; ++c) {
+                long idx = ((long)(b * 16 + c) << 12) + dn;
+                hstart[idx] = hs;
+                hs = Pst[idx] * hs + hend[idx];
+            }
+        } else if (gb < 64) {
+            int idx = (gb - 32) * 256 + tid;
+            int bc = idx >> 9, f = idx & 511;
+            float s = 0.f;
+            for (int t = 0; t < 128; ++t) {
+                long i = ((long)bc * 128 + t) * 512 + f;
+                s += b2f(Kp_hi[i]) + b2f(Kp_lo[i]);
+            }
+            dzc[(long)bc * 512 + f] = s;
+        } else {
+            int t = (gb - 64) * 256 + tid;
+            int b = t >> 17;
+            int df = t & 131071;
+            float acc = 0.f;
+            for (int c = 0; c < 8; ++c) {
+                long idx = (long)(b * 8 + c) * 131072 + df;
+                float v = dST_f[idx];
+                ushort_t h = f2b(acc);
+                ST_hi[idx] = h;
+                ST_lo[idx] = f2b(acc - b2f(h));
+                acc += v;
+            }
+        }
+    }
+    grid.sync();
+
     {
         GJob a{}; a.A0=scores_hi; a.A1=scores_lo; a.B0=VT_hi; a.B1=VT_lo;
         a.outF=numA_f; a.lda=128; a.ldb=1024; a.ldo=256;
@@ -712,43 +505,221 @@
         b.outF=numB_f; b.lda=512; b.ldb=512; b.ldo=256;
         b.act=ACT_NONE; b.ns=2; b.K=512; b.N=256; b.nx=4; b.ny=2; b.base=128; b.zmod=1;
         b.sAb1=65536; b.sBb1=131072; b.sOb=32768;
-        SJob s3{}; s3.x=x; s3.delta=delta_f; s3.BtCt=BtCt_f; s3.A_log=A_log;
-        s3.hstart=hstart; s3.giH=gatein_hi; s3.giL=gatein_lo; s3.base=256;
-        gemm_multi<2,3><<<dim3(768), T256, 0, stream>>>(a, b, jz, jz, jz, s3);
-    }
-    attn_finish<<<dim3(2048), dim3(64), 0, stream>>>(scores_f, Qp_hi, Qp_lo, dzc,
-        numA_f, numB_f, mbuf, ypre_hi, ypre_lo, gatein_hi, gatein_lo);
+        GJob js[2] = {a, b};
+        for (int vb = bid; vb < 768; vb += NB) {
+            if (vb >= 256)
+                ssm_body<3>(vb - 256, A.x, delta_f, BtCt_f, A.A_log, nullptr, nullptr,
+                            hstart, gatein_hi, gatein_lo, ldsbuf);
+            else
+                gemm_body<2>(vb, js, 2, ldsbuf);
+        }
+    }
+    grid.sync();
+
+    for (int v = bid; v < 512; v += NB) {
+        int w = tid >> 6, lane = tid & 63;
+        int token = v * 4 + w;
+        int b = token >> 10, tloc = token & 1023;
+        int c = tloc >> 7, tin = tloc & 127;
+        int bc = b * 8 + c;
+        const float* srow = scores_f + ((long)bc * 128 + tin) * 128;
+        float s = srow[lane] + srow[lane + 64];
+        const ushort_t* qh = Qp_hi + (long)token * 512;
+        const ushort_t* ql = Qp_lo + (long)token * 512;
+        float q[8];
+        #pragma unroll
+        for (int j = 0; j < 8; ++j) {
+            int f = lane + 64 * j;
+            q[j] = b2f(qh[f]) + b2f(ql[f]);
+        }
+        for (int c2 = 0; c2 < c; ++c2) {
+            const float* z = dzc + (long)(b * 8 + c2) * 512;
+            #pragma unroll
+            for (int j = 0; j < 8; ++j) s += q[j] * z[lane + 64 * j];
+        }
+        #pragma unroll
+        for (int m = 32; m; m >>= 1) s += __shfl_xor(s, m, 64);
+        float inv = 1.f / (s + 1e-6f);
+        const float* na = numA_f + (long)token * 256;
+        const float* nb = numB_f + (long)token * 256;
+        #pragma unroll
+        for (int j = 0; j < 4; ++j) {
+            int idx = lane + 64 * j;
+            float vv = (na[idx] + nb[idx]) * inv;
+            ushort_t h = f2b(vv);
+            ypre_hi[(long)token * 256 + idx] = h;
+            ypre_lo[(long)token * 256 + idx] = f2b(vv - b2f(h));
+        }
+        if (lane == 0) {
+            float wv[8];
+            #pragma unroll
+            for (int i = 0; i < 8; ++i) {
+                int idx = tloc - 7 + i;
+                wv[i] = (idx >= 0) ? mbuf[b * 1024 + idx] : -1e30f;
+            }
+            float mx = wv[0];
+            #pragma unroll
+            for (int i = 1; i < 8; ++i) mx = fmaxf(mx, wv[i]);
+            float e[8], sum = 0.f;
+            #pragma unroll
+            for (int i = 0; i < 8; ++i) { e[i] = __expf(wv[i] - mx); sum += e[i]; }
+            float invs = 1.f / sum, Hv = 0.f;
+            #pragma unroll
+            for (int i = 0; i < 8; ++i) {
+                float p = e[i] * invs;
+                Hv -= p * __logf(p + 1e-9f);
+            }
+            float H = Hv * 1.4426950408889634f;
+            ushort_t hh = f2b(H);
+            gatein_hi[(long)token * 576 + 512] = hh;
+            gatein_lo[(long)token * 576 + 512] = f2b(H - b2f(hh));
+        }
+        if (lane < 63) {
+            gatein_hi[(long)token * 576 + 513 + lane] = 0;
+            gatein_lo[(long)token * 576 + 513 + lane] = 0;
+        }
+    }
+    grid.sync();
+
     {
         GJob w{}; w.A0=ypre_hi; w.A1=ypre_lo; w.B0=WoT0; w.B1=WoT1;
         w.o0=gatein_hi; w.o1=gatein_lo; w.colOffB=256;
         w.lda=256; w.ldb=256; w.ldob=576;
         w.act=ACT_NONE; w.ns=2; w.K=256; w.N=256; w.nx=4; w.ny=32; w.base=0; w.zmod=1;
-        gemm_multi<2,0><<<dim3(128), T256, 0, stream>>>(w, jz, jz, jz, jz, sz);
-    }
-    {
-        GJob g{}; g.A0=gatein_hi; g.A1=gatein_lo; g.B0=Wg1T0; g.B1=Wg1T1; g.bias=bg1;
+        GJob js[1] = {w};
+        for (int v = bid; v < 128; v += NB) gemm_body<2>(v, js, 1, ldsbuf);
+    }
+    grid.sync();
+
+    {
+        GJob g{}; g.A0=gatein_hi; g.A1=gatein_lo; g.B0=Wg1T0; g.B1=Wg1T1; g.bias=A.bg1;
         g.o0=g1_hi; g.o1=g1_lo; g.lda=576; g.ldb=576; g.ldob=256;
         g.act=ACT_SILU; g.ns=2; g.K=576; g.N=256; g.nx=4; g.ny=32; g.base=0; g.zmod=1;
-        gemm_multi<2,0><<<dim3(128), T256, 0, stream>>>(g, jz, jz, jz, jz, sz);
-    }
-    {
-        GJob g{}; g.A0=g1_hi; g.A1=g1_lo; g.B0=Wg2T0; g.B1=Wg2T1; g.bias=bg2;
+        GJob js[1] = {g};
+        for (int v = bid; v < 128; v += NB) gemm_body<2>(v, js, 1, ldsbuf);
+    }
+    grid.sync();
+
+    {
+        GJob g{}; g.A0=g1_hi; g.A1=g1_lo; g.B0=Wg2T0; g.B1=Wg2T1; g.bias=A.bg2;
         g.outF=gbuf_f; g.lda=256; g.ldb=256; g.ldo=256;
         g.act=ACT_SIGMOID; g.ns=2; g.K=256; g.N=256; g.nx=4; g.ny=32; g.base=0; g.zmod=1;
-        gemm_multi<2,0><<<dim3(128), T256, 0, stream>>>(g, jz, jz, jz, jz, sz);
-    }
-    ln1_kernel<<<dim3(2048), T256, 0, stream>>>(x, gbuf_f, gatein_hi, gatein_lo, ln1_g, ln1_b, hbuf_f, hbuf_b);
-    {
-        GJob f{}; f.A0=hbuf_b; f.B0=Wf1T; f.bias=bf1;
+        GJob js[1] = {g};
+        for (int v = bid; v < 128; v += NB) gemm_body<2>(v, js, 1, ldsbuf);
+    }
+    grid.sync();
+
+    for (int t = bid; t < 2048; t += NB) {
+        float* red = (float*)ldsbuf;
+        long idx = (long)t * 256 + tid;
+        float yssm  = b2f(gatein_hi[(long)t * 576 + tid])       + b2f(gatein_lo[(long)t * 576 + tid]);
+        float yattn = b2f(gatein_hi[(long)t * 576 + 256 + tid]) + b2f(gatein_lo[(long)t * 576 + 256 + tid]);
+        float gv = gbuf_f[idx];
+        float v = A.x[idx] + gv * yssm + (1.f - gv) * yattn;
+        float s = v;
+        #pragma unroll
+        for (int m = 32; m; m >>= 1) s += __shfl_xor(s, m, 64);
+        if ((tid & 63) == 0) red[tid >> 6] = s;
+        __syncthreads();
+        float mu = (red[0] + red[1] + red[2] + red[3]) * (1.f / 256.f);
+        float dv = v - mu;
+        float s2 = dv * dv;
+        #pragma unroll
+        for (int m = 32; m; m >>= 1) s2 += __shfl_xor(s2, m, 64);
+        if ((tid & 63) == 0) red[4 + (tid >> 6)] = s2;
+        __syncthreads();
+        float var = (red[4] + red[5] + red[6] + red[7]) * (1.f / 256.f);
+        float o = dv * rsqrtf(var + 1e-5f) * A.ln1g[tid] + A.ln1b[tid];
+        hbuf_f[idx] = o;
+        hbuf_b[idx] = f2b(o);
+        __syncthreads();
+    }
+    grid.sync();
+
+    {
+        GJob f{}; f.A0=hbuf_b; f.B0=Wf1T; f.bias=A.bf1;
         f.o0=ffn1_b; f.lda=256; f.ldb=256; f.ldob=1024;
         f.act=ACT_GELU; f.ns=1; f.K=256; f.N=1024; f.nx=16; f.ny=32; f.base=0; f.zmod=1;
-        gemm_multi<1,0><<<dim3(512), T256, 0, stream>>>(f, jz, jz, jz, jz, sz);
-    }
-    {
-        GJob f{}; f.A0=ffn1_b; f.B0=Wf2T; f.bias=bf2;
+        GJob js[1] = {f};
+        for (int v = bid; v < 512; v += NB) gemm_body<1>(v, js, 1, ldsbuf);
+    }
+    grid.sync();
+
+    {
+        GJob f{}; f.A0=ffn1_b; f.B0=Wf2T; f.bias=A.bf2;
         f.outF=ffn2_f; f.lda=1024; f.ldb=1024; f.ldo=256;
         f.act=ACT_NONE; f.ns=1; f.K=1024; f.N=256; f.nx=4; f.ny=32; f.base=0; f.zmod=1;
-        gemm_multi<1,0><<<dim3(128), T256, 0, stream>>>(f, jz, jz, jz, jz, sz);
-    }
-    ln2_kernel<<<dim3(2048), T256, 0, stream>>>(hbuf_f, ffn2_f, ln2_g, ln2_b, out);
-}
+        GJob js[1] = {f};
+        for (int v = bid; v < 128; v += NB) gemm_body<1>(v, js, 1, ldsbuf);
+    }
+    grid.sync();
+
+    for (int t = bid; t < 2048; t += NB) {
+        float* red = (float*)ldsbuf;
+        long idx = (long)t * 256 + tid;
+        float v = hbuf_f[idx] + ffn2_f[idx];
+        float s = v;
+        #pragma unroll
+        for (int m = 32; m; m >>= 1) s += __shfl_xor(s, m, 64);
+        if ((tid & 63) == 0) red[tid >> 6] = s;
+        __syncthreads();
+        float mu = (red[0] + red[1] + red[2] + red[3]) * (1.f / 256.f);
+        float dv = v - mu;
+        float s2 = dv * dv;
+        #pragma unroll
+        for (int m = 32; m; m >>= 1) s2 += __shfl_xor(s2, m, 64);
+        if ((tid & 63) == 0) red[4 + (tid >> 6)] = s2;
+        __syncthreads();
+        float var = (red[4] + red[5] + red[6] + red[7]) * (1.f / 256.f);
+        A.out[idx] = dv * rsqrtf(var + 1e-5f) * A.ln2g[tid] + A.ln2b[tid];
+        __syncthreads();
+    }
+}
+
+
+extern "C" void kernel_launch(void* const* d_in, const int* in_sizes, int n_in,
+                              void* d_out, int out_size, void* d_ws, size_t ws_size,
+                              hipStream_t stream)
+{
+    if (ws_size < (size_t)42778624) return;
+
+    MegaArgs A;
+    A.x     = (const float*)d_in[0];
+    A.A_log = (const float*)d_in[1];
+    A.Wxp   = (const float*)d_in[2];
+    A.Wdt   = (const float*)d_in[3];
+    A.b_dt  = (const float*)d_in[4];
+    A.Wc    = (const float*)d_in[5];
+    A.Wq    = (const float*)d_in[6];
+    A.Wk    = (const float*)d_in[7];
+    A.Wv    = (const float*)d_in[8];
+    A.Wo    = (const float*)d_in[9];
+    A.omega = (const float*)d_in[10];
+    A.Wg1   = (const float*)d_in[11];
+    A.bg1   = (const float*)d_in[12];
+    A.Wg2   = (const float*)d_in[13];
+    A.bg2   = (const float*)d_in[14];
+    A.ln1g  = (const float*)d_in[15];
+    A.ln1b  = (const float*)d_in[16];
+    A.ln2g  = (const float*)d_in[17];
+    A.ln2b  = (const float*)d_in[18];
+    A.Wf1   = (const float*)d_in[19];
+    A.bf1   = (const float*)d_in[20];
+    A.Wf2   = (const float*)d_in[21];
+    A.bf2   = (const float*)d_in[22];
+    A.B     = (char*)d_ws;
+    A.out   = (float*)d_out;
+
+    int perCU = 0;
+    hipError_t qe = hipOccupancyMaxActiveBlocksPerMultiprocessor(
+        &perCU, (const void*)mega, 256, 0);
+    int grid = (qe == hipSuccess && perCU >= 2) ? 512 : 256;
+
+    void* kargs[] = { &A };
+    hipError_t le = hipLaunchCooperativeKernel((const void*)mega, dim3(grid),
+                                               dim3(256), kargs, 0, stream);
+    if (le != hipSuccess && grid != 256) {
+        hipLaunchCooperativeKernel((const void*)mega, dim3(256),
+                                   dim3(256), kargs, 0, stream);
+    }
+}
```

New measurement: 844.4 us. +170.8%, slower.
